# Performance work log

Measured on AMD Instinct MI355X. Metric: run time of the kernel, lower is better.

## Reference

```python
import jax, jax.numpy as jnp
import numpy as np

N = 6144          # active voxels / points
C = 96            # embed_channels
B = 2             # batch size
D = H = W = 32    # sparse spatial shape
K = 16            # PFAS kNN
DEPTH = 4
GRID_OPTS = np.array([[0.1, 0.1, 0.1], [0.4, 0.4, 0.4], [0.2, 0.2, 0.2]], dtype=np.float32)
BN_EPS = 1e-5


def _bn(x, g, b):
    # BatchNorm1d in training mode: batch stats over the point dim, biased var
    m = x.mean(0)
    v = jnp.var(x, axis=0)
    return (x - m) * jax.lax.rsqrt(v + BN_EPS) * g + b


def _seg_sum(x, seg):
    return jax.ops.segment_sum(x, seg, num_segments=N)


def _forward(indices, x, fp_w, fp_b, fp_g, fp_be, att_w1, att_b1, att_w2, att_b2,
             ff_w1, ff_b1, ff_g, ff_be, ff_w2, ff_b2, sa_w1, sa_b1, sa_w2, sa_b2,
             fj_w1, fj_b1, fj_g, fj_be, fj_w2, fj_b2,
             proj_w, proj_g, proj_be, lw_w, lw_g, lw_be, w_w, adp_w,
             fuse_w, fuse_g, fuse_be, conv1_w, bn1_g, bn1_be, conv2_w, bn2_g, bn2_be):
    # ---- CMPFE ----
    p = jax.nn.relu(_bn(x @ fp_w.T + fp_b, fp_g, fp_be))            # [N,9]
    cd, cl, nm = p[:, :3], p[:, 3:6], p[:, 6:9]

    def _att(f, i):
        h = jax.nn.relu(f @ att_w1[i].T + att_b1[i])
        return jax.nn.sigmoid(h @ att_w2[i].T + att_b2[i])

    enh = jnp.concatenate([cd, cl * _att(cl, 0), nm * _att(nm, 1)], axis=1)
    fu = jax.nn.relu(_bn(enh @ ff_w1.T + ff_b1, ff_g, ff_be)) @ ff_w2.T + ff_b2
    sem = jax.nn.sigmoid(jax.nn.relu(fu @ sa_w1.T + sa_b1) @ sa_w2.T + sa_b2)
    feat = fu * sem + x * (1.0 - sem)                               # new x.features

    # ---- PFAS: kNN geometry stats ----
    coord = indices[:, 1:].astype(jnp.float32)                      # [N,3]
    batch = indices[:, 0]
    sq = jnp.sum(coord * coord, axis=1)
    d2 = sq[:, None] + sq[None, :] - 2.0 * (coord @ coord.T)
    dist = jnp.sqrt(jnp.maximum(d2, 1e-12))
    same = batch[None, :] == batch[:, None]
    eye = jnp.eye(N, dtype=bool)
    dist = jnp.where(same & ~eye, dist, jnp.inf)
    neg_nd, idx = jax.lax.top_k(-dist, K)                           # K nearest
    nbr = coord[idx]                                                # [N,K,3]
    cent = nbr - nbr.mean(axis=1, keepdims=True)
    cov = jnp.einsum('nkd,nke->nde', cent, cent) / (K - 1)
    S = jnp.linalg.svd(cov, compute_uv=False)                       # [N,3] descending
    Sn = S / (S.sum(axis=1, keepdims=True) + 1e-6)
    linearity = Sn[:, 0:1] - (Sn[:, 1] + Sn[:, 2])[:, None]
    mean_dist = (-neg_nd).mean(axis=1, keepdims=True)
    density = 1.0 / (mean_dist + 1e-6)
    fl = jax.nn.relu(_bn(feat @ fj_w1.T + fj_b1, fj_g, fj_be)) @ fj_w2.T + fj_b2
    fp_ = jax.nn.softmax(fl, axis=1)
    tower = (density * 2.0 + fp_[:, 0:1]) / 3.0
    backg = (jnp.maximum(1.0 - linearity, 1.0 - density) + fp_[:, 1:2]) / 3.0
    line = (linearity * 2.0 + fp_[:, 2:3]) / 3.0
    go = jnp.asarray(GRID_OPTS)
    lg = go[2] * jnp.array([1.0, 1.0, 5.0], jnp.float32)            # last dim *5
    grid_sizes = tower * go[0] + backg * go[1] + line * lg + 1e-6   # [N,3]

    # ---- representative grids (N > 200 path) ----
    gm = grid_sizes.mean(axis=1)
    order = jnp.argsort(gm)
    reps = [grid_sizes[order[100:200]].mean(0),
            grid_sizes[order[::-1][:100]].mean(0),
            grid_sizes[order[:100]].mean(0)]

    # ---- voxel-grid clustering (torch_geometric voxel_grid + unique inverse) ----
    start = coord.min(axis=0)

    def _cluster(size):
        size = jnp.clip(size, 1e-6, None)
        c = jnp.clip(jnp.floor((coord - start) / size).astype(jnp.int64), 0, 4095)
        mx = c.max(axis=0) + 1
        ids = ((batch.astype(jnp.int64) * mx[0] + c[:, 0]) * mx[1] + c[:, 1]) * mx[2] + c[:, 2]
        _, inv = jnp.unique(ids, return_inverse=True, size=N, fill_value=0)
        return inv.reshape(-1)

    # ---- adaptive multi-branch scatter softmax aggregation ----
    branch_feats = []
    for i in range(DEPTH - 1):
        seg = _cluster(reps[i])
        cnt = jnp.maximum(_seg_sum(jnp.ones((N, 1), feat.dtype), seg), 1.0)
        pw = jax.nn.relu(_bn(feat @ lw_w[i].T, lw_g[i], lw_be[i]))
        pw = pw - (_seg_sum(pw, seg) / cnt)[seg]
        pw = pw @ w_w[i].T
        pw = jnp.exp(pw - pw.max())
        pw = pw / (_seg_sum(pw, seg)[seg] + 1e-6)
        pf = jax.nn.relu(_bn(feat @ proj_w[i].T, proj_g[i], proj_be[i])) * pw
        branch_feats.append(_seg_sum(pf, seg)[seg])
    adp = jax.nn.softmax(feat @ adp_w.T, axis=1)                    # [N,3]
    agg = jnp.einsum('nc,ncd->nd', adp, jnp.stack(branch_feats, 1))
    last = jax.nn.relu(_bn(feat @ proj_w[-1].T, proj_g[-1], proj_be[-1]))
    fused = jax.nn.relu(_bn(jnp.concatenate([last, agg], 1) @ fuse_w.T, fuse_g, fuse_be)) + feat
    res = fused

    # ---- submanifold sparse conv block (dense scatter form; inactive sites zero,
    #      outputs gathered only at active sites == SubMConv3d) ----
    bi, zi, yi, xi = indices[:, 0], indices[:, 1], indices[:, 2], indices[:, 3]

    def _subm(f, w):
        grid = jnp.zeros((B, D, H, W, C), f.dtype).at[bi, zi, yi, xi].set(f)
        o = jax.lax.conv_general_dilated(grid, w, (1, 1, 1), 'SAME',
                                         dimension_numbers=('NDHWC', 'DHWIO', 'NDHWC'))
        return o[bi, zi, yi, xi]

    f1 = jax.nn.relu(_bn(_subm(fused, conv1_w), bn1_g, bn1_be))
    f2 = _bn(_subm(f1, conv2_w), bn2_g, bn2_be)
    return jax.nn.relu(f2 + res)


def setup_inputs() -> dict:
    key = jax.random.key(0)
    ks = iter(jax.random.split(key, 64))

    def rn(*shape, s=0.05):
        return jax.random.normal(next(ks), shape, jnp.float32) * s

    # unique active voxel coordinates
    rng = np.random.default_rng(0)
    flat = rng.choice(B * D * H * W, size=N, replace=False)
    b = flat // (D * H * W)
    r = flat % (D * H * W)
    z = r // (H * W)
    y = (r % (H * W)) // W
    xw = r % W
    indices = jnp.asarray(np.stack([b, z, y, xw], 1).astype(np.int32))
    Ch = C // 2
    return {
        'x': jax.random.normal(next(ks), (N, C), jnp.float32),
        'indices': indices,
        'fp_w': rn(9, C), 'fp_b': rn(9), 'fp_g': jnp.ones(9), 'fp_be': jnp.zeros(9),
        'att_w1': rn(2, 16, 3), 'att_b1': rn(2, 16), 'att_w2': rn(2, 3, 16), 'att_b2': rn(2, 3),
        'ff_w1': rn(C, 9), 'ff_b1': rn(C), 'ff_g': jnp.ones(C), 'ff_be': jnp.zeros(C),
        'ff_w2': rn(C, C), 'ff_b2': rn(C),
        'sa_w1': rn(Ch, C), 'sa_b1': rn(Ch), 'sa_w2': rn(1, Ch), 'sa_b2': rn(1),
        'fj_w1': rn(64, C), 'fj_b1': rn(64), 'fj_g': jnp.ones(64), 'fj_be': jnp.zeros(64),
        'fj_w2': rn(3, 64), 'fj_b2': rn(3),
        'proj_w': rn(DEPTH, C, C), 'proj_g': jnp.ones((DEPTH, C)), 'proj_be': jnp.zeros((DEPTH, C)),
        'lw_w': rn(DEPTH - 1, C, C), 'lw_g': jnp.ones((DEPTH - 1, C)), 'lw_be': jnp.zeros((DEPTH - 1, C)),
        'w_w': rn(DEPTH - 1, C, C),
        'adp_w': rn(DEPTH - 1, C),
        'fuse_w': rn(C, 2 * C), 'fuse_g': jnp.ones(C), 'fuse_be': jnp.zeros(C),
        'conv1_w': rn(3, 3, 3, C, C), 'bn1_g': jnp.ones(C), 'bn1_be': jnp.zeros(C),
        'conv2_w': rn(3, 3, 3, C, C), 'bn2_g': jnp.ones(C), 'bn2_be': jnp.zeros(C),
    }


def reference(x, indices, fp_w, fp_b, fp_g, fp_be, att_w1, att_b1, att_w2, att_b2,
              ff_w1, ff_b1, ff_g, ff_be, ff_w2, ff_b2, sa_w1, sa_b1, sa_w2, sa_b2,
              fj_w1, fj_b1, fj_g, fj_be, fj_w2, fj_b2,
              proj_w, proj_g, proj_be, lw_w, lw_g, lw_be, w_w, adp_w,
              fuse_w, fuse_g, fuse_be, conv1_w, bn1_g, bn1_be, conv2_w, bn2_g, bn2_be):
    return _forward(indices, x, fp_w, fp_b, fp_g, fp_be, att_w1, att_b1, att_w2, att_b2,
                    ff_w1, ff_b1, ff_g, ff_be, ff_w2, ff_b2, sa_w1, sa_b1, sa_w2, sa_b2,
                    fj_w1, fj_b1, fj_g, fj_be, fj_w2, fj_b2,
                    proj_w, proj_g, proj_be, lw_w, lw_g, lw_be, w_w, adp_w,
                    fuse_w, fuse_g, fuse_be, conv1_w, bn1_g, bn1_be, conv2_w, bn2_g, bn2_be)
```

## Files before the change

### kernel.cpp

```cpp
#include <hip/hip_runtime.h>
#include <cstdint>

#define NPTS 6144
#define CH 96
#define NCELEM (NPTS*CH)
#define HTSZ 16384
#define NBALL 514

__device__ __forceinline__ unsigned fenc(float f){
  unsigned u = __float_as_uint(f);
  return (u & 0x80000000u) ? ~u : (u | 0x80000000u);
}
__device__ __forceinline__ float fdec(unsigned u){
  unsigned b = (u & 0x80000000u) ? (u & 0x7FFFFFFFu) : ~u;
  return __uint_as_float(b);
}

__device__ void eig3(double a00,double a01,double a02,double a11,double a12,double a22,
                     double &e0,double &e1,double &e2){
  double p1 = a01*a01 + a02*a02 + a12*a12;
  double q = (a00+a11+a22)/3.0;
  double b00=a00-q, b11=a11-q, b22=a22-q;
  double p2 = b00*b00 + b11*b11 + b22*b22 + 2.0*p1;
  if (p2 <= 1e-300){ e0=e1=e2=q; return; }
  double pp = sqrt(p2/6.0);
  double inv = 1.0/pp;
  double c00=b00*inv, c01=a01*inv, c02=a02*inv, c11=b11*inv, c12=a12*inv, c22=b22*inv;
  double det = c00*(c11*c22-c12*c12) - c01*(c01*c22-c12*c02) + c02*(c01*c12-c11*c02);
  double r = det*0.5;
  r = r < -1.0 ? -1.0 : (r > 1.0 ? 1.0 : r);
  double phi = acos(r)/3.0;
  e0 = q + 2.0*pp*cos(phi);
  e2 = q + 2.0*pp*cos(phi + 2.0943951023931953);
  e1 = 3.0*q - e0 - e2;
}

__global__ void k_setup0(int* __restrict__ zb, long zcount,
                         unsigned long long* __restrict__ htk, int* __restrict__ htv,
                         int* __restrict__ table, int* __restrict__ startmm){
  long i = (long)blockIdx.x*blockDim.x + threadIdx.x;
  long st = (long)gridDim.x*blockDim.x;
  for (long j=i; j<zcount; j+=st) zb[j] = 0;
  for (long j=i; j<3*HTSZ; j+=st){ htk[j] = ~0ull; htv[j] = 0x7fffffff; }
  for (long j=i; j<2*32768; j+=st) table[j] = -1;
  if (i < 3) startmm[i] = 0x7fffffff;
  else if (i < 6) startmm[i] = 0;
}
__global__ void __launch_bounds__(256) k_setup1(const int* __restrict__ ind,
                                                unsigned* __restrict__ packed,
                                                int* __restrict__ startmm,
                                                int* __restrict__ table,
                                                unsigned* __restrict__ ball){
  __shared__ int mn[3], mx[3];
  __shared__ int hcnt[32], hbase[32], hpos[32];
  int tid = threadIdx.x;
  if (blockIdx.x < 24){
    if (tid < 3){ mn[tid] = 0x7fffffff; mx[tid] = 0; }
    __syncthreads();
    int p = blockIdx.x*256 + tid;
    int b = ind[p*4], z = ind[p*4+1], y = ind[p*4+2], x = ind[p*4+3];
    packed[p] = (unsigned)((b<<15)|(z<<10)|(y<<5)|x);
    table[((b*32+z)*32+y)*32+x] = p;
    atomicMin(&mn[0], z); atomicMin(&mn[1], y); atomicMin(&mn[2], x);
    atomicMax(&mx[0], z); atomicMax(&mx[1], y); atomicMax(&mx[2], x);
    __syncthreads();
    if (tid < 3){
      atomicMin(&startmm[tid], mn[tid]);
      atomicMax(&startmm[3+tid], mx[tid]);
    }
  } else {
    if (tid < 32){ hcnt[tid] = 0; hpos[tid] = 0; }
    __syncthreads();
    for (int i=tid; i<1331; i+=256){
      int dz = i/121, rm = i - dz*121, dy = rm/11, dx = rm - dy*11;
      int a = dz-5, b = dy-5, c = dx-5;
      int d2 = a*a + b*b + c*c;
      if (d2 > 0 && d2 <= 25) atomicAdd(&hcnt[d2], 1);
    }
    __syncthreads();
    if (tid == 0){
      int acc = 0;
      for (int d=1; d<=25; ++d){ hbase[d] = acc; acc += hcnt[d]; }
    }
    __syncthreads();
    for (int i=tid; i<1331; i+=256){
      int dz = i/121, rm = i - dz*121, dy = rm/11, dx = rm - dy*11;
      int a = dz-5, b = dy-5, c = dx-5;
      int d2 = a*a + b*b + c*c;
      if (d2 > 0 && d2 <= 25){
        int pos = hbase[d2] + atomicAdd(&hpos[d2], 1);
        ball[pos] = ((unsigned)d2<<16)|((unsigned)dz<<10)|((unsigned)dy<<5)|(unsigned)dx;
      }
    }
  }
}

__global__ void __launch_bounds__(256) k_mm(
    const float* __restrict__ Abase, const float* __restrict__ Wbase,
    const float* __restrict__ biasBase, float* __restrict__ Obase,
    int CIN, int COUT,
    long sA, long sW, long sO, long sBias,
    const float* __restrict__ statsBase, long sStats,
    const float* __restrict__ gBase, const float* __restrict__ beBase, long sGB,
    const float* __restrict__ SsumBase, const int* __restrict__ segBase, const int* __restrict__ cntBase,
    unsigned* maxenc, int mode)
{
  int zb = blockIdx.y;
  const float* A = Abase + (long)zb*sA;
  const float* W = Wbase + (long)zb*sW;
  float* O = Obase + (long)zb*sO;
  const float* st = statsBase ? statsBase + (long)zb*sStats : nullptr;
  const float* g  = gBase ? gBase + (long)zb*sGB : nullptr;
  const float* be = beBase ? beBase + (long)zb*sGB : nullptr;
  const float* Ss = SsumBase ? SsumBase + (long)zb*NCELEM : nullptr;
  const int* seg  = segBase ? segBase + (long)zb*NPTS : nullptr;
  const int* cnt  = cntBase ? cntBase + (long)zb*NPTS : nullptr;

  __shared__ float Alt[96*34];
  __shared__ float Wlt[96*98];
  int tid = threadIdx.x;
  int r0 = blockIdx.x*32;
  for (int idx = tid; idx < CIN*COUT; idx += 256){
    int co = idx / CIN, k = idx - co*CIN;
    Wlt[k*98 + co] = W[idx];
  }
  for (int idx = tid; idx < 32*CIN; idx += 256){
    int ir = idx / CIN, k = idx - ir*CIN;
    int row = r0 + ir;
    float v = A[(long)row*CIN + k];
    if (mode >= 1) v = fmaxf((v - st[k*2])*st[k*2+1]*g[k] + be[k], 0.f);
    if (mode == 2){
      int s = seg[row];
      float cf = fmaxf((float)cnt[s], 1.f);
      v -= Ss[(long)s*CH + k] / cf;
    }
    Alt[k*34 + ir] = v;
  }
  __syncthreads();
  float lmax = -3.4e38f;
  if (COUT == 96){
    int rp = tid >> 4, cg = tid & 15;
    int co0 = cg*6;
    float acc0[6], acc1[6];
    #pragma unroll
    for (int j=0;j<6;++j){
      float b = biasBase ? biasBase[(long)zb*sBias + co0 + j] : 0.f;
      acc0[j] = b; acc1[j] = b;
    }
    int ra = 2*rp;
    for (int k=0;k<CIN;++k){
      float2 a  = *(const float2*)&Alt[k*34 + ra];
      float2 w0 = *(const float2*)&Wlt[k*98 + co0];
      float2 w1 = *(const float2*)&Wlt[k*98 + co0 + 2];
      float2 w2 = *(const float2*)&Wlt[k*98 + co0 + 4];
      acc0[0] = fmaf(a.x, w0.x, acc0[0]); acc1[0] = fmaf(a.y, w0.x, acc1[0]);
      acc0[1] = fmaf(a.x, w0.y, acc0[1]); acc1[1] = fmaf(a.y, w0.y, acc1[1]);
      acc0[2] = fmaf(a.x, w1.x, acc0[2]); acc1[2] = fmaf(a.y, w1.x, acc1[2]);
      acc0[3] = fmaf(a.x, w1.y, acc0[3]); acc1[3] = fmaf(a.y, w1.y, acc1[3]);
      acc0[4] = fmaf(a.x, w2.x, acc0[4]); acc1[4] = fmaf(a.y, w2.x, acc1[4]);
      acc0[5] = fmaf(a.x, w2.y, acc0[5]); acc1[5] = fmaf(a.y, w2.y, acc1[5]);
    }
    int rb = ra+1;
    #pragma unroll
    for (int j=0;j<6;++j){
      O[(long)(r0+ra)*96 + co0 + j] = acc0[j];
      O[(long)(r0+rb)*96 + co0 + j] = acc1[j];
      lmax = fmaxf(lmax, fmaxf(acc0[j], acc1[j]));
    }
  } else {
    for (int idx = tid; idx < 32*COUT; idx += 256){
      int ir = idx/COUT, co = idx - ir*COUT;
      float acc = biasBase ? biasBase[(long)zb*sBias + co] : 0.f;
      for (int k=0;k<CIN;++k) acc = fmaf(Alt[k*34+ir], Wlt[k*98+co], acc);
      O[(long)(r0+ir)*COUT + co] = acc;
      lmax = fmaxf(lmax, acc);
    }
  }
  if (maxenc){
    __shared__ float rmx[256];
    rmx[tid] = lmax; __syncthreads();
    for (int s2=128; s2>0; s2>>=1){
      if (tid < s2) rmx[tid] = fmaxf(rmx[tid], rmx[tid+s2]);
      __syncthreads();
    }
    if (tid == 0) atomicMax(&maxenc[zb], fenc(rmx[0]));
  }
}

__global__ void __launch_bounds__(256) k_mm_fuse(
    const float* __restrict__ tp3, const float* __restrict__ st,
    const float* __restrict__ pg3, const float* __restrict__ pbe3,
    const float* __restrict__ agg, const float* __restrict__ fw, float* __restrict__ tf)
{
  __shared__ float Alt[192*34];
  __shared__ float Wlt[96*98];
  int tid = threadIdx.x, r0 = blockIdx.x*32;
  for (int idx = tid; idx < 32*192; idx += 256){
    int ir = idx/192, k = idx - ir*192;
    int row = r0 + ir;
    float v;
    if (k < 96){
      v = tp3[(long)row*96 + k];
      v = fmaxf((v - st[k*2])*st[k*2+1]*pg3[k] + pbe3[k], 0.f);
    } else {
      v = agg[(long)row*96 + (k-96)];
    }
    Alt[k*34 + ir] = v;
  }
  int rp = tid >> 4, cg = tid & 15, co0 = cg*6;
  float acc0[6] = {0,0,0,0,0,0}, acc1[6] = {0,0,0,0,0,0};
  int ra = 2*rp, rb = ra+1;
  for (int h=0; h<2; ++h){
    __syncthreads();
    for (int idx = tid; idx < 96*96; idx += 256){
      int co = idx/96, k = idx - co*96;
      Wlt[k*98+co] = fw[(long)co*192 + h*96 + k];
    }
    __syncthreads();
    for (int k=0;k<96;++k){
      float2 a  = *(const float2*)&Alt[(h*96 + k)*34 + ra];
      float2 w0 = *(const float2*)&Wlt[k*98 + co0];
      float2 w1 = *(const float2*)&Wlt[k*98 + co0 + 2];
      float2 w2 = *(const float2*)&Wlt[k*98 + co0 + 4];
      acc0[0] = fmaf(a.x, w0.x, acc0[0]); acc1[0] = fmaf(a.y, w0.x, acc1[0]);
      acc0[1] = fmaf(a.x, w0.y, acc0[1]); acc1[1] = fmaf(a.y, w0.y, acc1[1]);
      acc0[2] = fmaf(a.x, w1.x, acc0[2]); acc1[2] = fmaf(a.y, w1.x, acc1[2]);
      acc0[3] = fmaf(a.x, w1.y, acc0[3]); acc1[3] = fmaf(a.y, w1.y, acc1[3]);
      acc0[4] = fmaf(a.x, w2.x, acc0[4]); acc1[4] = fmaf(a.y, w2.x, acc1[4]);
      acc0[5] = fmaf(a.x, w2.y, acc0[5]); acc1[5] = fmaf(a.y, w2.y, acc1[5]);
    }
  }
  #pragma unroll
  for (int j=0;j<6;++j){
    tf[(long)(r0+ra)*96 + co0 + j] = acc0[j];
    tf[(long)(r0+rb)*96 + co0 + j] = acc1[j];
  }
}

__global__ void k_stats(const float* __restrict__ Abase, long sA, int COLS,
                        float* __restrict__ statsBase, long sStats){
  int col = blockIdx.x, zb = blockIdx.y;
  const float* A = Abase + (long)zb*sA;
  double s = 0.0, q = 0.0;
  for (int r = threadIdx.x; r < NPTS; r += 256){
    double v = (double)A[(long)r*COLS + col];
    s += v; q += v*v;
  }
  __shared__ double ls[256], lq[256];
  ls[threadIdx.x] = s; lq[threadIdx.x] = q; __syncthreads();
  for (int t=128; t>0; t>>=1){
    if (threadIdx.x < t){ ls[threadIdx.x] += ls[threadIdx.x+t]; lq[threadIdx.x] += lq[threadIdx.x+t]; }
    __syncthreads();
  }
  if (threadIdx.x == 0){
    double mean = ls[0]/NPTS;
    double var = lq[0]/NPTS - mean*mean;
    float* stp = statsBase + (long)zb*sStats + col*2;
    stp[0] = (float)mean;
    stp[1] = (float)(1.0/sqrt(var + 1e-5));
  }
}

__global__ void k_p_att_enh(const float* __restrict__ t9, const float* __restrict__ st,
                            const float* __restrict__ fg, const float* __restrict__ fbe,
                            const float* __restrict__ aw1, const float* __restrict__ ab1,
                            const float* __restrict__ aw2, const float* __restrict__ ab2,
                            float* __restrict__ enh){
  int p = blockIdx.x*blockDim.x + threadIdx.x;
  if (p >= NPTS) return;
  float pp[9];
  #pragma unroll
  for (int c=0;c<9;++c){
    float v = t9[p*9+c];
    pp[c] = fmaxf((v - st[c*2])*st[c*2+1]*fg[c] + fbe[c], 0.f);
  }
  float eo[9];
  eo[0]=pp[0]; eo[1]=pp[1]; eo[2]=pp[2];
  #pragma unroll
  for (int i=0;i<2;++i){
    const float* w1 = aw1 + i*48;
    const float* b1 = ab1 + i*16;
    const float* w2 = aw2 + i*48;
    const float* b2 = ab2 + i*3;
    const float* f = pp + 3 + i*3;
    float h[16];
    #pragma unroll
    for (int j=0;j<16;++j){
      float s = b1[j];
      #pragma unroll
      for (int k=0;k<3;++k) s = fmaf(f[k], w1[j*3+k], s);
      h[j] = fmaxf(s, 0.f);
    }
    #pragma unroll
    for (int o=0;o<3;++o){
      float s = b2[o];
      #pragma unroll
      for (int j=0;j<16;++j) s = fmaf(h[j], w2[o*16+j], s);
      float a = 1.f/(1.f + expf(-s));
      eo[3+i*3+o] = f[o]*a;
    }
  }
  #pragma unroll
  for (int c=0;c<9;++c) enh[p*9+c] = eo[c];
}

__global__ void __launch_bounds__(256) k_sem_feat(
    const float* __restrict__ fu, const float* __restrict__ x,
    const float* __restrict__ w1, const float* __restrict__ b1,
    const float* __restrict__ w2, const float* __restrict__ b2,
    float* __restrict__ feat){
  int wid = (blockIdx.x*blockDim.x + threadIdx.x) >> 6;
  int lane = threadIdx.x & 63;
  if (wid >= NPTS) return;
  const float* fr = fu + (long)wid*96;
  float partial = 0.f;
  if (lane < 48){
    float h = b1[lane];
    for (int k=0;k<96;++k) h = fmaf(fr[k], w1[lane*96+k], h);
    h = fmaxf(h, 0.f);
    partial = h * w2[lane];
  }
  for (int m=32; m; m>>=1) partial += __shfl_xor(partial, m);
  float sem = 1.f/(1.f + expf(-(partial + b2[0])));
  for (int c=lane; c<96; c+=64){
    float f = fr[c];
    feat[(long)wid*96+c] = f*sem + x[(long)wid*96+c]*(1.f - sem);
  }
}

__global__ void __launch_bounds__(256) k_knn(const unsigned* __restrict__ packed,
                                             const int* __restrict__ table,
                                             const unsigned* __restrict__ ball,
                                             float* __restrict__ density, float* __restrict__ linearity){
  __shared__ unsigned pk[NPTS];
  for (int i=threadIdx.x; i<NPTS; i+=256) pk[i] = packed[i];
  __syncthreads();
  int pid = blockIdx.x*4 + (threadIdx.x>>6);
  int lane = threadIdx.x & 63;
  unsigned mypc = pk[pid];
  int myb = (int)(mypc>>15);
  int mz = (int)((mypc>>10)&31), my_=(int)((mypc>>5)&31), mx_=(int)(mypc&31);
  unsigned s[16];
  #pragma unroll
  for (int t=0;t<16;++t) s[t] = 0xFFFFFFFFu;
  int cnt = 0;
  const int tbase = myb*32768;
  for (int it=0; it<9; ++it){
    int i = lane + it*64;
    if (i < NBALL){
      unsigned e = ball[i];
      int d2 = (int)(e >> 16);
      int dz = (int)((e>>10)&31) - 5;
      int dy = (int)((e>>5)&31) - 5;
      int dx = (int)(e&31) - 5;
      int zz = mz+dz, yy = my_+dy, xx = mx_+dx;
      if ((unsigned)zz < 32u && (unsigned)yy < 32u && (unsigned)xx < 32u){
        int j = table[tbase + (zz*32+yy)*32+xx];
        if (j >= 0){
          ++cnt;
          unsigned key = ((unsigned)d2<<13) | (unsigned)j;
          if (key < s[15]){
            s[15] = key;
            #pragma unroll
            for (int t=15;t>0;--t){
              unsigned a = s[t-1], b = s[t];
              unsigned lo = a<b?a:b, hi = a<b?b:a;
              s[t-1]=lo; s[t]=hi;
            }
          }
        }
      }
    }
    int nxt = (it+1)*64;
    if (nxt >= NBALL) break;
    int tot = cnt;
    for (int m=32; m; m>>=1) tot += __shfl_xor(tot, m);
    unsigned dlast = ball[nxt-1] >> 16;
    unsigned dnext = ball[nxt] >> 16;
    if (tot >= 16 && dnext > dlast) break;
  }
  int tot = cnt;
  for (int m=32; m; m>>=1) tot += __shfl_xor(tot, m);
  if (tot < 16){
    #pragma unroll
    for (int t=0;t<16;++t) s[t] = 0xFFFFFFFFu;
    for (int it=0; it<96; ++it){
      int j = lane + it*64;
      unsigned pc = pk[j];
      if (j != pid && (int)(pc>>15) == myb){
        int dz = (int)((pc>>10)&31) - mz;
        int dy = (int)((pc>>5)&31) - my_;
        int dx = (int)(pc&31) - mx_;
        unsigned d2 = (unsigned)(dz*dz + dy*dy + dx*dx);
        unsigned key = (d2<<13) | (unsigned)j;
        if (key < s[15]){
          s[15] = key;
          #pragma unroll
          for (int t=15;t>0;--t){
            unsigned a = s[t-1], b = s[t];
            unsigned lo = a<b?a:b, hi = a<b?b:a;
            s[t-1]=lo; s[t]=hi;
          }
        }
      }
    }
  }
  float sdist = 0.f;
  int sz=0,sy=0,sx=0,szz=0,syy=0,sxx=0,szy=0,szx=0,syx=0;
  for (int r=0;r<16;++r){
    unsigned m = s[0];
    #pragma unroll
    for (int w=32; w; w>>=1){
      unsigned o = (unsigned)__shfl_xor((int)m, w);
      m = m<o ? m : o;
    }
    bool own = (s[0] == m);
    #pragma unroll
    for (int t=0;t<15;++t) s[t] = own ? s[t+1] : s[t];
    if (own) s[15] = 0xFFFFFFFFu;
    unsigned idx = m & 8191u;
    unsigned d2 = m >> 13;
    sdist += sqrtf((float)d2);
    unsigned pc = pk[idx];
    int nz=(int)((pc>>10)&31), ny=(int)((pc>>5)&31), nx=(int)(pc&31);
    sz+=nz; sy+=ny; sx+=nx;
    szz+=nz*nz; syy+=ny*ny; sxx+=nx*nx; szy+=nz*ny; szx+=nz*nx; syx+=ny*nx;
  }
  if (lane == 0){
    double m0 = sz/16.0, m1 = sy/16.0, m2 = sx/16.0;
    float c00 = (float)(((double)szz - 16.0*m0*m0)/15.0);
    float c11 = (float)(((double)syy - 16.0*m1*m1)/15.0);
    float c22 = (float)(((double)sxx - 16.0*m2*m2)/15.0);
    float c01 = (float)(((double)szy - 16.0*m0*m1)/15.0);
    float c02 = (float)(((double)szx - 16.0*m0*m2)/15.0);
    float c12 = (float)(((double)syx - 16.0*m1*m2)/15.0);
    double e0,e1,e2;
    eig3((double)c00,(double)c01,(double)c02,(double)c11,(double)c12,(double)c22, e0,e1,e2);
    float s0 = (float)fabs(e0), s1 = (float)fabs(e1), s2 = (float)fabs(e2);
    float den = s0 + s1 + s2 + 1e-6f;
    float sn0 = s0/den, sn1 = s1/den, sn2 = s2/den;
    linearity[pid] = sn0 - (sn1 + sn2);
    float md = sdist * (1.f/16.f);
    density[pid] = 1.f/(md + 1e-6f);
  }
}

__global__ void k_geo(const float* __restrict__ t64, const float* __restrict__ st,
                      const float* __restrict__ fg, const float* __restrict__ fbe,
                      const float* __restrict__ w2, const float* __restrict__ b2,
                      const float* __restrict__ density, const float* __restrict__ linearity,
                      float* __restrict__ gsz, float* __restrict__ gm){
  int p = blockIdx.x*blockDim.x + threadIdx.x;
  if (p >= NPTS) return;
  float fl[3];
  #pragma unroll
  for (int o=0;o<3;++o) fl[o] = b2[o];
  for (int k=0;k<64;++k){
    float v = t64[(long)p*64+k];
    v = fmaxf((v - st[k*2])*st[k*2+1]*fg[k] + fbe[k], 0.f);
    #pragma unroll
    for (int o=0;o<3;++o) fl[o] = fmaf(v, w2[o*64+k], fl[o]);
  }
  float mx = fmaxf(fl[0], fmaxf(fl[1], fl[2]));
  float e0 = expf(fl[0]-mx), e1 = expf(fl[1]-mx), e2 = expf(fl[2]-mx);
  float es = e0+e1+e2;
  float p0 = e0/es, p1 = e1/es, p2 = e2/es;
  float den = density[p], lin = linearity[p];
  float tw = (den*2.f + p0)/3.f;
  float bg = (fmaxf(1.f-lin, 1.f-den) + p1)/3.f;
  float ln = (lin*2.f + p2)/3.f;
  float g0 = tw*0.1f + bg*0.4f + ln*0.2f + 1e-6f;
  float g1 = tw*0.1f + bg*0.4f + ln*0.2f + 1e-6f;
  float g2 = tw*0.1f + bg*0.4f + ln*1.0f + 1e-6f;
  gsz[p*3+0]=g0; gsz[p*3+1]=g1; gsz[p*3+2]=g2;
  gm[p] = (g0+g1+g2)/3.f;
}

#define RNKCHUNK 768
__global__ void __launch_bounds__(256) k_rank(const float* __restrict__ gm, int* __restrict__ rank){
  __shared__ unsigned long long lk[RNKCHUNK];
  int j0 = blockIdx.y*RNKCHUNK;
  for (int i=threadIdx.x; i<RNKCHUNK; i+=256){
    int j = j0 + i;
    lk[i] = (((unsigned long long)fenc(gm[j]))<<13) | (unsigned long long)j;
  }
  __syncthreads();
  int p = blockIdx.x*256 + threadIdx.x;
  unsigned long long myk = (((unsigned long long)fenc(gm[p]))<<13) | (unsigned long long)p;
  int cnt = 0;
  #pragma unroll 4
  for (int i=0; i<RNKCHUNK; ++i) cnt += (lk[i] < myk) ? 1 : 0;
  atomicAdd(&rank[p], cnt);
}
__global__ void __launch_bounds__(256) k_scatter_reps(const int* __restrict__ rank,
                                                      const float* __restrict__ gsz,
                                                      float* __restrict__ bkt,
                                                      int* __restrict__ done,
                                                      float* __restrict__ reps){
  __shared__ int lastf;
  int p = blockIdx.x*256 + threadIdx.x;
  int r = rank[p];
  int zb = -1, t = 0;
  if (r < 100){ zb = 2; t = r; }
  else if (r < 200){ zb = 0; t = r - 100; }
  else if (r >= NPTS-100){ zb = 1; t = r - (NPTS-100); }
  if (zb >= 0){
    #pragma unroll
    for (int d=0; d<3; ++d) bkt[(zb*100 + t)*3 + d] = gsz[p*3+d];
  }
  __threadfence();
  __syncthreads();
  if (threadIdx.x == 0) lastf = (atomicAdd(done, 1) == 23) ? 1 : 0;
  __syncthreads();
  if (lastf){
    __threadfence();
    int i = threadIdx.x;
    if (i < 9){
      int z = i/3, d = i - z*3;
      double s = 0.0;
      for (int tt=0; tt<100; ++tt) s += (double)bkt[(z*100 + tt)*3 + d];
      reps[i] = (float)(s/100.0);
    }
  }
}

__global__ void k_cluster(const int* __restrict__ ind, const float* __restrict__ reps,
                          const int* __restrict__ startmm, long long* __restrict__ ids){
  int z = blockIdx.y;
  int p = blockIdx.x*blockDim.x + threadIdx.x;
  if (p >= NPTS) return;
  long long mxp[3]; int cc[3];
  #pragma unroll
  for (int d=0; d<3; ++d){
    float sizev = fmaxf(reps[z*3+d], 1e-6f);
    float cf = floorf(((float)ind[p*4+1+d] - (float)startmm[d]) / sizev);
    int ci = (int)cf;
    ci = ci < 0 ? 0 : (ci > 4095 ? 4095 : ci);
    cc[d] = ci;
    float cfm = floorf(((float)startmm[3+d] - (float)startmm[d]) / sizev);
    int cm = (int)cfm;
    cm = cm < 0 ? 0 : (cm > 4095 ? 4095 : cm);
    mxp[d] = (long long)cm + 1;
  }
  long long b = ind[p*4];
  ids[(long)z*NPTS + p] = ((b*mxp[0] + cc[0])*mxp[1] + cc[1])*mxp[2] + cc[2];
}

__device__ __forceinline__ int ht_hash(unsigned long long id){
  unsigned long long h = id * 0x9E3779B97F4A7C15ull;
  return (int)(h >> 49) & (HTSZ-1);
}
__global__ void k_seg_build(const long long* __restrict__ ids,
                            unsigned long long* __restrict__ keys, int* __restrict__ vals){
  int z = blockIdx.y;
  int p = blockIdx.x*blockDim.x + threadIdx.x;
  if (p >= NPTS) return;
  unsigned long long id = (unsigned long long)ids[(long)z*NPTS + p];
  unsigned long long* K = keys + (long)z*HTSZ;
  int* V = vals + (long)z*HTSZ;
  int slot = ht_hash(id);
  while (true){
    unsigned long long prev = atomicCAS(&K[slot], ~0ull, id);
    if (prev == ~0ull || prev == id){ atomicMin(&V[slot], p); break; }
    slot = (slot + 1) & (HTSZ-1);
  }
}
__global__ void k_seg_lookup(const long long* __restrict__ ids,
                             const unsigned long long* __restrict__ keys, const int* __restrict__ vals,
                             int* __restrict__ seg, int* __restrict__ cnt){
  int z = blockIdx.y;
  int p = blockIdx.x*blockDim.x + threadIdx.x;
  if (p >= NPTS) return;
  unsigned long long id = (unsigned long long)ids[(long)z*NPTS + p];
  const unsigned long long* K = keys + (long)z*HTSZ;
  int slot = ht_hash(id);
  while (K[slot] != id) slot = (slot + 1) & (HTSZ-1);
  int rep = vals[(long)z*HTSZ + slot];
  seg[(long)z*NPTS + p] = rep;
  atomicAdd(&cnt[(long)z*NPTS + rep], 1);
}

__global__ void k_pw_accum(const float* __restrict__ tlw, const float* __restrict__ stats,
                           const float* __restrict__ g, const float* __restrict__ be,
                           const int* __restrict__ seg, float* __restrict__ S){
  int z = blockIdx.y;
  int idx = blockIdx.x*blockDim.x + threadIdx.x;
  int p = idx/CH, c = idx - p*CH;
  const float* st = stats + z*192;
  float v = tlw[(long)z*NCELEM + idx];
  v = fmaxf((v - st[c*2])*st[c*2+1]*g[z*CH+c] + be[z*CH+c], 0.f);
  atomicAdd(&S[(long)z*NCELEM + (long)seg[(long)z*NPTS+p]*CH + c], v);
}
__global__ void k_exp_accum(const float* __restrict__ pw2, const unsigned* __restrict__ maxenc,
                            const int* __restrict__ seg, float* __restrict__ E){
  int z = blockIdx.y;
  int idx = blockIdx.x*blockDim.x + threadIdx.x;
  int p = idx/CH, c = idx - p*CH;
  float mv = fdec(maxenc[z]);
  float v = expf(pw2[(long)z*NCELEM + idx] - mv);
  atomicAdd(&E[(long)z*NCELEM + (long)seg[(long)z*NPTS+p]*CH + c], v);
}
__global__ void k_pf_accum(const float* __restrict__ tp, const float* __restrict__ stats,
                           const float* __restrict__ pg, const float* __restrict__ pbe,
                           const float* __restrict__ pw2, const unsigned* __restrict__ maxenc,
                           const int* __restrict__ seg, const float* __restrict__ E,
                           float* __restrict__ F){
  int z = blockIdx.y;
  int idx = blockIdx.x*blockDim.x + threadIdx.x;
  int p = idx/CH, c = idx - p*CH;
  const float* st = stats + z*192;
  float v = tp[(long)z*NCELEM + idx];
  v = fmaxf((v - st[c*2])*st[c*2+1]*pg[z*CH+c] + pbe[z*CH+c], 0.f);
  float mv = fdec(maxenc[z]);
  int sg = seg[(long)z*NPTS+p];
  float w = expf(pw2[(long)z*NCELEM + idx] - mv) / (E[(long)z*NCELEM + (long)sg*CH + c] + 1e-6f);
  atomicAdd(&F[(long)z*NCELEM + (long)sg*CH + c], v*w);
}
__global__ void __launch_bounds__(256) k_adp_agg(
    const float* __restrict__ feat, const float* __restrict__ aw,
    const float* __restrict__ F, const int* __restrict__ seg,
    float* __restrict__ agg){
  __shared__ float ladp[32][3];
  __shared__ int lseg[32][3];
  int tid = threadIdx.x;
  int p0 = blockIdx.x*32;
  if (tid < 96){
    int pl = tid/3, z = tid - pl*3;
    const float* fr = feat + (long)(p0+pl)*CH;
    float a = 0.f;
    for (int k=0;k<CH;++k) a = fmaf(fr[k], aw[z*CH+k], a);
    ladp[pl][z] = a;
    lseg[pl][z] = seg[(long)z*NPTS + (p0+pl)];
  }
  __syncthreads();
  if (tid < 32){
    float a0 = ladp[tid][0], a1 = ladp[tid][1], a2 = ladp[tid][2];
    float m = fmaxf(a0, fmaxf(a1,a2));
    float e0 = expf(a0-m), e1 = expf(a1-m), e2 = expf(a2-m);
    float s = e0+e1+e2;
    ladp[tid][0]=e0/s; ladp[tid][1]=e1/s; ladp[tid][2]=e2/s;
  }
  __syncthreads();
  for (int e = tid; e < 32*CH; e += 256){
    int pl = e/CH, c = e - pl*CH;
    float s = 0.f;
    #pragma unroll
    for (int z=0;z<3;++z)
      s = fmaf(ladp[pl][z], F[(long)z*NCELEM + (long)lseg[pl][z]*CH + c], s);
    agg[(long)p0*CH + e] = s;
  }
}

__global__ void k_zero(int* p, long n){
  long i = (long)blockIdx.x*blockDim.x + threadIdx.x;
  long st = (long)gridDim.x*blockDim.x;
  for (; i < n; i += st) p[i] = 0;
}
__global__ void k_fused(const float* __restrict__ tf, const float* __restrict__ st,
                        const float* __restrict__ fg, const float* __restrict__ fbe,
                        const float* __restrict__ feat, float* __restrict__ fused){
  int idx = blockIdx.x*blockDim.x + threadIdx.x;
  int c = idx % CH;
  float v = tf[idx];
  v = fmaxf((v - st[c*2])*st[c*2+1]*fg[c] + fbe[c], 0.f);
  fused[idx] = v + feat[idx];
}
__global__ void k_bnrelu(const float* __restrict__ a, const float* __restrict__ st,
                         const float* __restrict__ g, const float* __restrict__ be,
                         float* __restrict__ o){
  int idx = blockIdx.x*blockDim.x + threadIdx.x;
  int c = idx % CH;
  float v = a[idx];
  o[idx] = fmaxf((v - st[c*2])*st[c*2+1]*g[c] + be[c], 0.f);
}

__global__ void __launch_bounds__(256) k_nbrlist(const int* __restrict__ ind,
                                                 const int* __restrict__ table,
                                                 int* __restrict__ nbrtab,
                                                 int* __restrict__ tapcnt,
                                                 int* __restrict__ ptlist){
  __shared__ int pb[256], pz[256], py[256], px[256];
  __shared__ int lcnt[27], lbase[27], lpos[27];
  int tid = threadIdx.x;
  if (tid < 27){ lcnt[tid] = 0; lpos[tid] = 0; }
  int p0 = blockIdx.x*256;
  pb[tid] = ind[(p0+tid)*4];
  pz[tid] = ind[(p0+tid)*4+1];
  py[tid] = ind[(p0+tid)*4+2];
  px[tid] = ind[(p0+tid)*4+3];
  __syncthreads();
  int base = blockIdx.x*6912;
  int qv[27];
  #pragma unroll 1
  for (int j = 0; j < 27; ++j){
    int i = tid + j*256;
    int pl = i/27, tap = i - pl*27;
    int dz = tap/9 - 1;
    int rm = tap % 9;
    int dy = rm/3 - 1, dx = rm%3 - 1;
    int z = pz[pl]+dz, y = py[pl]+dy, x = px[pl]+dx;
    int q = -1;
    if ((unsigned)z < 32u && (unsigned)y < 32u && (unsigned)x < 32u)
      q = table[((pb[pl]*32+z)*32+y)*32+x];
    qv[j] = q;
    nbrtab[base + i] = q;
    if (q >= 0) atomicAdd(&lcnt[tap], 1);
  }
  __syncthreads();
  if (tid < 27) lbase[tid] = atomicAdd(&tapcnt[tid], lcnt[tid]);
  __syncthreads();
  #pragma unroll 1
  for (int j = 0; j < 27; ++j){
    int q = qv[j];
    if (q >= 0){
      int i = tid + j*256;
      int tap = i % 27;
      int p = p0 + i/27;
      int pos = lbase[tap] + atomicAdd(&lpos[tap], 1);
      ptlist[tap*NPTS + pos] = (p<<16) | q;
    }
  }
}
__global__ void __launch_bounds__(256) k_conv_gemm(
    const float* __restrict__ src, const float* __restrict__ Wc,
    const int* __restrict__ tapcnt, const int* __restrict__ ptlist,
    const float* __restrict__ bnst, const float* __restrict__ bng,
    const float* __restrict__ bnbe, const float* __restrict__ res,
    int fmode, float* __restrict__ part){
  int tap = blockIdx.y;
  int n = tapcnt[tap];
  int r0 = blockIdx.x*32;
  if (r0 >= n) return;
  __shared__ float Alt[96*34];
  __shared__ float Wlt[96*98];
  __shared__ int pqs[32];
  int tid = threadIdx.x;
  if (tid < 32){
    int r = r0 + tid;
    pqs[tid] = (r < n) ? ptlist[tap*NPTS + r] : -1;
  }
  __syncthreads();
  for (int idx4 = tid; idx4 < 2304; idx4 += 256){
    int ci = idx4/24, c4 = idx4 - ci*24;
    float4 w = ((const float4*)(Wc + ((long)tap*96 + ci)*96))[c4];
    float* d = &Wlt[ci*98 + c4*4];
    d[0]=w.x; d[1]=w.y; d[2]=w.z; d[3]=w.w;
  }
  for (int idx4 = tid; idx4 < 32*24; idx4 += 256){
    int ir = idx4/24, c4 = idx4 - ir*24;
    int pq = pqs[ir];
    float4 s4 = make_float4(0.f,0.f,0.f,0.f);
    if (pq >= 0){
      int q = pq & 0xFFFF;
      s4 = ((const float4*)(src + (long)q*CH))[c4];
      if (fmode){
        int c0 = c4*4;
        float vx = fmaxf((s4.x - bnst[(c0+0)*2])*bnst[(c0+0)*2+1]*bng[c0+0] + bnbe[c0+0], 0.f);
        float vy = fmaxf((s4.y - bnst[(c0+1)*2])*bnst[(c0+1)*2+1]*bng[c0+1] + bnbe[c0+1], 0.f);
        float vz = fmaxf((s4.z - bnst[(c0+2)*2])*bnst[(c0+2)*2+1]*bng[c0+2] + bnbe[c0+2], 0.f);
        float vw = fmaxf((s4.w - bnst[(c0+3)*2])*bnst[(c0+3)*2+1]*bng[c0+3] + bnbe[c0+3], 0.f);
        if (fmode == 2){
          const float* rr = res + (long)q*CH + c0;
          vx += rr[0]; vy += rr[1]; vz += rr[2]; vw += rr[3];
        }
        s4 = make_float4(vx,vy,vz,vw);
      }
    }
    int k0 = c4*4;
    Alt[(k0+0)*34 + ir] = s4.x;
    Alt[(k0+1)*34 + ir] = s4.y;
    Alt[(k0+2)*34 + ir] = s4.z;
    Alt[(k0+3)*34 + ir] = s4.w;
  }
  __syncthreads();
  int rp = tid >> 4, cg = tid & 15;
  int co0 = cg*6;
  int ra = 2*rp, rb = ra+1;
  float acc0[6]={0,0,0,0,0,0}, acc1[6]={0,0,0,0,0,0};
  for (int k=0;k<96;++k){
    float2 a  = *(const float2*)&Alt[k*34 + ra];
    float2 w0 = *(const float2*)&Wlt[k*98 + co0];
    float2 w1 = *(const float2*)&Wlt[k*98 + co0 + 2];
    float2 w2 = *(const float2*)&Wlt[k*98 + co0 + 4];
    acc0[0] = fmaf(a.x, w0.x, acc0[0]); acc1[0] = fmaf(a.y, w0.x, acc1[0]);
    acc0[1] = fmaf(a.x, w0.y, acc0[1]); acc1[1] = fmaf(a.y, w0.y, acc1[1]);
    acc0[2] = fmaf(a.x, w1.x, acc0[2]); acc1[2] = fmaf(a.y, w1.x, acc1[2]);
    acc0[3] = fmaf(a.x, w1.y, acc0[3]); acc1[3] = fmaf(a.y, w1.y, acc1[3]);
    acc0[4] = fmaf(a.x, w2.x, acc0[4]); acc1[4] = fmaf(a.y, w2.x, acc1[4]);
    acc0[5] = fmaf(a.x, w2.y, acc0[5]); acc1[5] = fmaf(a.y, w2.y, acc1[5]);
  }
  int pa = pqs[ra], pb2 = pqs[rb];
  if (pa >= 0){
    float* o = part + ((long)(pa>>16)*27 + tap)*CH + co0;
    #pragma unroll
    for (int j=0;j<6;++j) o[j] = acc0[j];
  }
  if (pb2 >= 0){
    float* o = part + ((long)(pb2>>16)*27 + tap)*CH + co0;
    #pragma unroll
    for (int j=0;j<6;++j) o[j] = acc1[j];
  }
}
__global__ void __launch_bounds__(256) k_conv_sum(const int* __restrict__ nbrtab,
                                                  const float* __restrict__ part,
                                                  float* __restrict__ out){
  int idx = blockIdx.x*256 + threadIdx.x;
  int p = idx/24, c4 = idx - p*24;
  const int* nt = nbrtab + p*27;
  float4 acc = make_float4(0.f,0.f,0.f,0.f);
  for (int tap=0; tap<27; ++tap){
    if (nt[tap] >= 0){
      float4 v = ((const float4*)part)[((long)p*27 + tap)*24 + c4];
      acc.x += v.x; acc.y += v.y; acc.z += v.z; acc.w += v.w;
    }
  }
  ((float4*)out)[idx] = acc;
}
__global__ void __launch_bounds__(256) k_conv_gemm_atomic(
    const float* __restrict__ src, const float* __restrict__ Wc,
    const int* __restrict__ tapcnt, const int* __restrict__ ptlist,
    float* __restrict__ out){
  int tap = blockIdx.y;
  int n = tapcnt[tap];
  int r0 = blockIdx.x*32;
  if (r0 >= n) return;
  __shared__ float Al[32*97];
  __shared__ float Wl[96*97];
  __shared__ int pqs[32];
  int tid = threadIdx.x;
  if (tid < 32){
    int r = r0 + tid;
    pqs[tid] = (r < n) ? ptlist[tap*NPTS + r] : -1;
  }
  __syncthreads();
  for (int idx4 = tid; idx4 < 2304; idx4 += 256){
    int ci = idx4/24, c4 = idx4 - ci*24;
    float4 w = ((const float4*)(Wc + ((long)tap*96 + ci)*96))[c4];
    float* d = &Wl[ci*97 + c4*4];
    d[0]=w.x; d[1]=w.y; d[2]=w.z; d[3]=w.w;
  }
  for (int idx4 = tid; idx4 < 32*24; idx4 += 256){
    int ir = idx4/24, c4 = idx4 - ir*24;
    int pq = pqs[ir];
    float4 s = make_float4(0.f,0.f,0.f,0.f);
    if (pq >= 0){
      int q = pq & 0xFFFF;
      s = ((const float4*)(src + (long)q*CH))[c4];
    }
    float* d = &Al[ir*97 + c4*4];
    d[0]=s.x; d[1]=s.y; d[2]=s.z; d[3]=s.w;
  }
  __syncthreads();
  int rp = tid >> 4, cg = tid & 15;
  int co0 = cg*6;
  int ra = 2*rp, rb = ra+1;
  float acc0[6]={0,0,0,0,0,0}, acc1[6]={0,0,0,0,0,0};
  for (int k=0;k<96;++k){
    float a0 = Al[ra*97+k], a1 = Al[rb*97+k];
    #pragma unroll
    for (int j=0;j<6;++j){
      float w = Wl[k*97+co0+j];
      acc0[j] = fmaf(a0, w, acc0[j]);
      acc1[j] = fmaf(a1, w, acc1[j]);
    }
  }
  int pa = pqs[ra], pb = pqs[rb];
  if (pa >= 0){
    float* o = out + (long)(pa>>16)*CH + co0;
    #pragma unroll
    for (int j=0;j<6;++j) atomicAdd(&o[j], acc0[j]);
  }
  if (pb >= 0){
    float* o = out + (long)(pb>>16)*CH + co0;
    #pragma unroll
    for (int j=0;j<6;++j) atomicAdd(&o[j], acc1[j]);
  }
}
__global__ void k_final(const float* __restrict__ c2, const float* __restrict__ st12,
                        const float* __restrict__ g2, const float* __restrict__ be2,
                        const float* __restrict__ tf, const float* __restrict__ st10,
                        const float* __restrict__ fg, const float* __restrict__ fbe,
                        const float* __restrict__ feat, float* __restrict__ out){
  int idx = blockIdx.x*blockDim.x + threadIdx.x;
  int c = idx % CH;
  float fsd = fmaxf((tf[idx] - st10[c*2])*st10[c*2+1]*fg[c] + fbe[c], 0.f) + feat[idx];
  float v = (c2[idx] - st12[c*2])*st12[c*2+1]*g2[c] + be2[c];
  out[idx] = fmaxf(v + fsd, 0.f);
}

extern "C" void kernel_launch(void* const* d_in, const int* in_sizes, int n_in,
                              void* d_out, int out_size, void* d_ws, size_t ws_size,
                              hipStream_t stream)
{
  const float* x      = (const float*)d_in[0];
  const int*   ind    = (const int*)  d_in[1];
  const float* fp_w   = (const float*)d_in[2];
  const float* fp_b   = (const float*)d_in[3];
  const float* fp_g   = (const float*)d_in[4];
  const float* fp_be  = (const float*)d_in[5];
  const float* att_w1 = (const float*)d_in[6];
  const float* att_b1 = (const float*)d_in[7];
  const float* att_w2 = (const float*)d_in[8];
  const float* att_b2 = (const float*)d_in[9];
  const float* ff_w1  = (const float*)d_in[10];
  const float* ff_b1  = (const float*)d_in[11];
  const float* ff_g   = (const float*)d_in[12];
  const float* ff_be  = (const float*)d_in[13];
  const float* ff_w2  = (const float*)d_in[14];
  const float* ff_b2  = (const float*)d_in[15];
  const float* sa_w1  = (const float*)d_in[16];
  const float* sa_b1  = (const float*)d_in[17];
  const float* sa_w2  = (const float*)d_in[18];
  const float* sa_b2  = (const float*)d_in[19];
  const float* fj_w1  = (const float*)d_in[20];
  const float* fj_b1  = (const float*)d_in[21];
  const float* fj_g   = (const float*)d_in[22];
  const float* fj_be  = (const float*)d_in[23];
  const float* fj_w2  = (const float*)d_in[24];
  const float* fj_b2  = (const float*)d_in[25];
  const float* proj_w = (const float*)d_in[26];
  const float* proj_g = (const float*)d_in[27];
  const float* proj_be= (const float*)d_in[28];
  const float* lw_w   = (const float*)d_in[29];
  const float* lw_g   = (const float*)d_in[30];
  const float* lw_be  = (const float*)d_in[31];
  const float* w_w    = (const float*)d_in[32];
  const float* adp_w  = (const float*)d_in[33];
  const float* fuse_w = (const float*)d_in[34];
  const float* fuse_g = (const float*)d_in[35];
  const float* fuse_be= (const float*)d_in[36];
  const float* conv1_w= (const float*)d_in[37];
  const float* bn1_g  = (const float*)d_in[38];
  const float* bn1_be = (const float*)d_in[39];
  const float* conv2_w= (const float*)d_in[40];
  const float* bn2_g  = (const float*)d_in[41];
  const float* bn2_be = (const float*)d_in[42];
  float* outp = (float*)d_out;
  (void)in_sizes; (void)n_in; (void)out_size;

  char* ws = (char*)d_ws;
  size_t off = 0;
  auto alloc = [&](size_t bytes)->size_t{
    off = (off + 255) & ~(size_t)255;
    size_t o = off; off += bytes; return o;
  };
  const size_t FNC = (size_t)NCELEM*4;
  size_t o_packed = alloc((size_t)NPTS*4);
  size_t o_start  = alloc(32);
  size_t o_ball   = alloc((size_t)NBALL*4);
  size_t o_dens   = alloc((size_t)NPTS*4);
  size_t o_lin    = alloc((size_t)NPTS*4);
  size_t o_t9     = alloc((size_t)NPTS*9*4);
  size_t o_enh    = alloc((size_t)NPTS*9*4);
  size_t o_gm     = alloc((size_t)NPTS*4);
  size_t o_gsz    = alloc((size_t)NPTS*3*4);
  size_t o_reps   = alloc(16*4);
  size_t o_bkt    = alloc((size_t)3*100*3*4);
  size_t o_ids    = alloc((size_t)3*NPTS*8);
  size_t o_seg    = alloc((size_t)3*NPTS*4);
  size_t o_table  = alloc((size_t)65536*4);
  size_t o_nbr    = alloc((size_t)NPTS*27*4);
  size_t o_ptlist = alloc((size_t)27*NPTS*4);
  size_t o_t64    = alloc((size_t)NPTS*64*4);
  size_t o_stats  = alloc((size_t)13*192*4);
  size_t o_htk    = alloc((size_t)3*HTSZ*8);
  size_t o_htv    = alloc((size_t)3*HTSZ*4);
  size_t o_S      = alloc(3*FNC);
  size_t o_E      = alloc(3*FNC);
  size_t o_F      = alloc(3*FNC);
  size_t o_cnt    = alloc((size_t)3*NPTS*4);
  size_t o_rank   = alloc((size_t)NPTS*4);
  size_t o_tapcnt = alloc(32*4);
  size_t o_done   = alloc(16);
  size_t o_maxenc = alloc(16*4);
  size_t zend = off;
  size_t o_T96 = alloc(FNC);
  size_t o_fu  = alloc(FNC);
  size_t o_feat= alloc(FNC);
  size_t o_tlw = alloc(3*FNC);
  size_t o_pw2 = alloc(3*FNC);
  size_t o_tp  = alloc(4*FNC);
  size_t o_agg = alloc(FNC);
  size_t o_tf  = alloc(FNC);
  size_t o_fsd = alloc(FNC);
  size_t o_c1  = alloc(FNC);
  size_t o_f1  = alloc(FNC);
  size_t o_c2  = alloc(FNC);
  size_t o_part = alloc((size_t)NPTS*27*CH*4);
  bool use_part = (off <= ws_size);

  float* stats = (float*)(ws + o_stats);
  long zcount = (long)((zend - o_S)/4);

  k_setup0<<<dim3(2048), dim3(256), 0, stream>>>((int*)(ws+o_S), zcount,
      (unsigned long long*)(ws+o_htk), (int*)(ws+o_htv), (int*)(ws+o_table), (int*)(ws+o_start));
  k_setup1<<<dim3(25), 256, 0, stream>>>(ind, (unsigned*)(ws+o_packed),
      (int*)(ws+o_start), (int*)(ws+o_table), (unsigned*)(ws+o_ball));

  k_mm<<<dim3(192,1), 256, 0, stream>>>(x, fp_w, fp_b, (float*)(ws+o_t9), 96, 9,
      0,0,0,0, nullptr,0, nullptr,nullptr,0, nullptr,nullptr,nullptr, nullptr, 0);
  k_stats<<<dim3(9,1), 256, 0, stream>>>((float*)(ws+o_t9), 0, 9, stats+0*192, 0);
  k_p_att_enh<<<dim3(24), 256, 0, stream>>>((float*)(ws+o_t9), stats+0*192, fp_g, fp_be,
      att_w1, att_b1, att_w2, att_b2, (float*)(ws+o_enh));

  k_mm<<<dim3(192,1), 256, 0, stream>>>((float*)(ws+o_enh), ff_w1, ff_b1, (float*)(ws+o_T96), 9, 96,
      0,0,0,0, nullptr,0, nullptr,nullptr,0, nullptr,nullptr,nullptr, nullptr, 0);
  k_stats<<<dim3(96,1), 256, 0, stream>>>((float*)(ws+o_T96), 0, 96, stats+1*192, 0);
  k_mm<<<dim3(192,1), 256, 0, stream>>>((float*)(ws+o_T96), ff_w2, ff_b2, (float*)(ws+o_fu), 96, 96,
      0,0,0,0, stats+1*192,0, ff_g, ff_be,0, nullptr,nullptr,nullptr, nullptr, 1);

  k_sem_feat<<<dim3(1536), 256, 0, stream>>>((float*)(ws+o_fu), x, sa_w1, sa_b1, sa_w2, sa_b2,
      (float*)(ws+o_feat));

  k_knn<<<dim3(1536), 256, 0, stream>>>((unsigned*)(ws+o_packed), (int*)(ws+o_table),
      (unsigned*)(ws+o_ball), (float*)(ws+o_dens), (float*)(ws+o_lin));

  k_mm<<<dim3(192,1), 256, 0, stream>>>((float*)(ws+o_feat), fj_w1, fj_b1, (float*)(ws+o_t64), 96, 64,
      0,0,0,0, nullptr,0, nullptr,nullptr,0, nullptr,nullptr,nullptr, nullptr, 0);
  k_stats<<<dim3(64,1), 256, 0, stream>>>((float*)(ws+o_t64), 0, 64, stats+2*192, 0);
  k_geo<<<dim3(24), 256, 0, stream>>>((float*)(ws+o_t64), stats+2*192, fj_g, fj_be, fj_w2, fj_b2,
      (float*)(ws+o_dens), (float*)(ws+o_lin), (float*)(ws+o_gsz), (float*)(ws+o_gm));

  k_rank<<<dim3(24,8), 256, 0, stream>>>((float*)(ws+o_gm), (int*)(ws+o_rank));
  k_scatter_reps<<<dim3(24), 256, 0, stream>>>((int*)(ws+o_rank), (float*)(ws+o_gsz),
      (float*)(ws+o_bkt), (int*)(ws+o_done), (float*)(ws+o_reps));

  k_cluster<<<dim3(24,3), 256, 0, stream>>>(ind, (float*)(ws+o_reps), (int*)(ws+o_start),
      (long long*)(ws+o_ids));
  k_seg_build<<<dim3(24,3), 256, 0, stream>>>((long long*)(ws+o_ids),
      (unsigned long long*)(ws+o_htk), (int*)(ws+o_htv));
  k_seg_lookup<<<dim3(24,3), 256, 0, stream>>>((long long*)(ws+o_ids),
      (unsigned long long*)(ws+o_htk), (int*)(ws+o_htv), (int*)(ws+o_seg), (int*)(ws+o_cnt));

  k_mm<<<dim3(192,3), 256, 0, stream>>>((float*)(ws+o_feat), lw_w, nullptr, (float*)(ws+o_tlw), 96, 96,
      0, 96*96, NCELEM, 0, nullptr,0, nullptr,nullptr,0, nullptr,nullptr,nullptr, nullptr, 0);
  k_stats<<<dim3(96,3), 256, 0, stream>>>((float*)(ws+o_tlw), NCELEM, 96, stats+3*192, 192);
  k_pw_accum<<<dim3(2304,3), 256, 0, stream>>>((float*)(ws+o_tlw), stats+3*192, lw_g, lw_be,
      (int*)(ws+o_seg), (float*)(ws+o_S));
  k_mm<<<dim3(192,3), 256, 0, stream>>>((float*)(ws+o_tlw), w_w, nullptr, (float*)(ws+o_pw2), 96, 96,
      NCELEM, 96*96, NCELEM, 0, stats+3*192,192, lw_g, lw_be,96,
      (float*)(ws+o_S), (int*)(ws+o_seg), (int*)(ws+o_cnt), (unsigned*)(ws+o_maxenc), 2);
  k_exp_accum<<<dim3(2304,3), 256, 0, stream>>>((float*)(ws+o_pw2), (unsigned*)(ws+o_maxenc),
      (int*)(ws+o_seg), (float*)(ws+o_E));
  k_mm<<<dim3(192,4), 256, 0, stream>>>((float*)(ws+o_feat), proj_w, nullptr, (float*)(ws+o_tp), 96, 96,
      0, 96*96, NCELEM, 0, nullptr,0, nullptr,nullptr,0, nullptr,nullptr,nullptr, nullptr, 0);
  k_stats<<<dim3(96,4), 256, 0, stream>>>((float*)(ws+o_tp), NCELEM, 96, stats+6*192, 192);
  k_pf_accum<<<dim3(2304,3), 256, 0, stream>>>((float*)(ws+o_tp), stats+6*192, proj_g, proj_be,
      (float*)(ws+o_pw2), (unsigned*)(ws+o_maxenc), (int*)(ws+o_seg), (float*)(ws+o_E), (float*)(ws+o_F));
  k_adp_agg<<<dim3(192), 256, 0, stream>>>((float*)(ws+o_feat), adp_w, (float*)(ws+o_F),
      (int*)(ws+o_seg), (float*)(ws+o_agg));

  k_mm_fuse<<<dim3(192), 256, 0, stream>>>((float*)(ws+o_tp) + (size_t)3*NCELEM, stats+9*192,
      proj_g + 3*96, proj_be + 3*96, (float*)(ws+o_agg), fuse_w, (float*)(ws+o_tf));
  k_stats<<<dim3(96,1), 256, 0, stream>>>((float*)(ws+o_tf), 0, 96, stats+10*192, 0);

  k_nbrlist<<<dim3(24), 256, 0, stream>>>(ind, (int*)(ws+o_table), (int*)(ws+o_nbr),
      (int*)(ws+o_tapcnt), (int*)(ws+o_ptlist));
  if (use_part){
    k_conv_gemm<<<dim3(192,27), 256, 0, stream>>>((float*)(ws+o_tf), conv1_w,
        (int*)(ws+o_tapcnt), (int*)(ws+o_ptlist),
        stats+10*192, fuse_g, fuse_be, (float*)(ws+o_feat), 2, (float*)(ws+o_part));
    k_conv_sum<<<dim3(NPTS*24/256), 256, 0, stream>>>((int*)(ws+o_nbr), (float*)(ws+o_part),
        (float*)(ws+o_c1));
    k_stats<<<dim3(96,1), 256, 0, stream>>>((float*)(ws+o_c1), 0, 96, stats+11*192, 0);
    k_conv_gemm<<<dim3(192,27), 256, 0, stream>>>((float*)(ws+o_c1), conv2_w,
        (int*)(ws+o_tapcnt), (int*)(ws+o_ptlist),
        stats+11*192, bn1_g, bn1_be, nullptr, 1, (float*)(ws+o_part));
    k_conv_sum<<<dim3(NPTS*24/256), 256, 0, stream>>>((int*)(ws+o_nbr), (float*)(ws+o_part),
        (float*)(ws+o_c2));
  } else {
    k_fused<<<dim3(2304), 256, 0, stream>>>((float*)(ws+o_tf), stats+10*192, fuse_g, fuse_be,
        (float*)(ws+o_feat), (float*)(ws+o_fsd));
    k_zero<<<dim3(2304), dim3(256), 0, stream>>>((int*)(ws+o_c1), NCELEM);
    k_conv_gemm_atomic<<<dim3(192,27), 256, 0, stream>>>((float*)(ws+o_fsd), conv1_w,
        (int*)(ws+o_tapcnt), (int*)(ws+o_ptlist), (float*)(ws+o_c1));
    k_stats<<<dim3(96,1), 256, 0, stream>>>((float*)(ws+o_c1), 0, 96, stats+11*192, 0);
    k_bnrelu<<<dim3(2304), 256, 0, stream>>>((float*)(ws+o_c1), stats+11*192, bn1_g, bn1_be,
        (float*)(ws+o_f1));
    k_zero<<<dim3(2304), dim3(256), 0, stream>>>((int*)(ws+o_c2), NCELEM);
    k_conv_gemm_atomic<<<dim3(192,27), 256, 0, stream>>>((float*)(ws+o_f1), conv2_w,
        (int*)(ws+o_tapcnt), (int*)(ws+o_ptlist), (float*)(ws+o_c2));
  }
  k_stats<<<dim3(96,1), 256, 0, stream>>>((float*)(ws+o_c2), 0, 96, stats+12*192, 0);
  k_final<<<dim3(2304), 256, 0, stream>>>((float*)(ws+o_c2), stats+12*192, bn2_g, bn2_be,
      (float*)(ws+o_tf), stats+10*192, fuse_g, fuse_be, (float*)(ws+o_feat), outp);
}
```

Baseline: 486.6 us.

## Fuse BatchNorm statistic accumulation into producer GEMM epilogues and inline cluster ids

Removes most separate k_stats launches. The GEMM, fuse-GEMM and conv-sum kernels now accumulate per-channel sums and sums of squares, first in shared-memory float atomics and then in global double atomics. Consumers derive mean and rstd from the raw double sums and cache them in shared memory. The k_cluster kernel and its ids buffer are dropped, with cluster ids recomputed inside the hash build and lookup kernels. This saves launches and full re-reads of activations, at the cost of atomic contention and E[x^2]-mean^2 variance computed from per-block float partial sums.

New measurement: 516.7 us. +6.2%, slower.

```diff
diff --git a/kernel.cpp b/kernel.cpp
--- a/kernel.cpp
+++ b/kernel.cpp
@@ -14,6 +14,11 @@
 __device__ __forceinline__ float fdec(unsigned u){
   unsigned b = (u & 0x80000000u) ? (u & 0x7FFFFFFFu) : ~u;
   return __uint_as_float(b);
+}
+__device__ __forceinline__ float2 bnstat(const double* __restrict__ st, int c){
+  double mean = st[c*2] / (double)NPTS;
+  double var  = st[c*2+1] / (double)NPTS - mean*mean;
+  return make_float2((float)mean, (float)(1.0/sqrt(var + 1e-5)));
 }
 
 __device__ void eig3(double a00,double a01,double a02,double a11,double a12,double a22,
@@ -100,26 +105,35 @@
     const float* __restrict__ biasBase, float* __restrict__ Obase,
     int CIN, int COUT,
     long sA, long sW, long sO, long sBias,
-    const float* __restrict__ statsBase, long sStats,
+    const double* __restrict__ statsBase, long sStats,
     const float* __restrict__ gBase, const float* __restrict__ beBase, long sGB,
     const float* __restrict__ SsumBase, const int* __restrict__ segBase, const int* __restrict__ cntBase,
-    unsigned* maxenc, int mode)
+    unsigned* maxenc, int mode, double* statsumBase)
 {
   int zb = blockIdx.y;
   const float* A = Abase + (long)zb*sA;
   const float* W = Wbase + (long)zb*sW;
   float* O = Obase + (long)zb*sO;
-  const float* st = statsBase ? statsBase + (long)zb*sStats : nullptr;
+  const double* st = statsBase ? statsBase + (long)zb*sStats : nullptr;
   const float* g  = gBase ? gBase + (long)zb*sGB : nullptr;
   const float* be = beBase ? beBase + (long)zb*sGB : nullptr;
   const float* Ss = SsumBase ? SsumBase + (long)zb*NCELEM : nullptr;
   const int* seg  = segBase ? segBase + (long)zb*NPTS : nullptr;
   const int* cnt  = cntBase ? cntBase + (long)zb*NPTS : nullptr;
+  double* ssum = statsumBase ? statsumBase + (long)zb*192 : nullptr;
 
   __shared__ float Alt[96*34];
   __shared__ float Wlt[96*98];
+  __shared__ float lms[192];
+  __shared__ float lsum[96], lsq[96];
   int tid = threadIdx.x;
   int r0 = blockIdx.x*32;
+  if (tid < 96){ lsum[tid] = 0.f; lsq[tid] = 0.f; }
+  if (mode >= 1 && tid < CIN){
+    float2 ms = bnstat(st, tid);
+    lms[tid*2] = ms.x; lms[tid*2+1] = ms.y;
+  }
+  __syncthreads();
   for (int idx = tid; idx < CIN*COUT; idx += 256){
     int co = idx / CIN, k = idx - co*CIN;
     Wlt[k*98 + co] = W[idx];
@@ -128,7 +142,7 @@
     int ir = idx / CIN, k = idx - ir*CIN;
     int row = r0 + ir;
     float v = A[(long)row*CIN + k];
-    if (mode >= 1) v = fmaxf((v - st[k*2])*st[k*2+1]*g[k] + be[k], 0.f);
+    if (mode >= 1) v = fmaxf((v - lms[k*2])*lms[k*2+1]*g[k] + be[k], 0.f);
     if (mode == 2){
       int s = seg[row];
       float cf = fmaxf((float)cnt[s], 1.f);
@@ -167,6 +181,13 @@
       O[(long)(r0+rb)*96 + co0 + j] = acc1[j];
       lmax = fmaxf(lmax, fmaxf(acc0[j], acc1[j]));
     }
+    if (ssum){
+      #pragma unroll
+      for (int j=0;j<6;++j){
+        atomicAdd(&lsum[co0+j], acc0[j] + acc1[j]);
+        atomicAdd(&lsq[co0+j],  acc0[j]*acc0[j] + acc1[j]*acc1[j]);
+      }
+    }
   } else {
     for (int idx = tid; idx < 32*COUT; idx += 256){
       int ir = idx/COUT, co = idx - ir*COUT;
@@ -174,6 +195,17 @@
       for (int k=0;k<CIN;++k) acc = fmaf(Alt[k*34+ir], Wlt[k*98+co], acc);
       O[(long)(r0+ir)*COUT + co] = acc;
       lmax = fmaxf(lmax, acc);
+      if (ssum){
+        atomicAdd(&lsum[co], acc);
+        atomicAdd(&lsq[co], acc*acc);
+      }
+    }
+  }
+  if (ssum){
+    __syncthreads();
+    if (tid < COUT){
+      atomicAdd(&ssum[tid*2],   (double)lsum[tid]);
+      atomicAdd(&ssum[tid*2+1], (double)lsq[tid]);
     }
   }
   if (maxenc){
@@ -188,20 +220,27 @@
 }
 
 __global__ void __launch_bounds__(256) k_mm_fuse(
-    const float* __restrict__ tp3, const float* __restrict__ st,
+    const float* __restrict__ tp3, const double* __restrict__ st,
     const float* __restrict__ pg3, const float* __restrict__ pbe3,
-    const float* __restrict__ agg, const float* __restrict__ fw, float* __restrict__ tf)
+    const float* __restrict__ agg, const float* __restrict__ fw, float* __restrict__ tf,
+    double* __restrict__ tfsum)
 {
   __shared__ float Alt[192*34];
   __shared__ float Wlt[96*98];
+  __shared__ float lscr[192];
   int tid = threadIdx.x, r0 = blockIdx.x*32;
+  if (tid < 96){
+    float2 ms = bnstat(st, tid);
+    lscr[tid*2] = ms.x; lscr[tid*2+1] = ms.y;
+  }
+  __syncthreads();
   for (int idx = tid; idx < 32*192; idx += 256){
     int ir = idx/192, k = idx - ir*192;
     int row = r0 + ir;
     float v;
     if (k < 96){
       v = tp3[(long)row*96 + k];
-      v = fmaxf((v - st[k*2])*st[k*2+1]*pg3[k] + pbe3[k], 0.f);
+      v = fmaxf((v - lscr[k*2])*lscr[k*2+1]*pg3[k] + pbe3[k], 0.f);
     } else {
       v = agg[(long)row*96 + (k-96)];
     }
@@ -235,10 +274,23 @@
     tf[(long)(r0+ra)*96 + co0 + j] = acc0[j];
     tf[(long)(r0+rb)*96 + co0 + j] = acc1[j];
   }
+  __syncthreads();
+  if (tid < 96){ lscr[tid] = 0.f; lscr[96+tid] = 0.f; }
+  __syncthreads();
+  #pragma unroll
+  for (int j=0;j<6;++j){
+    atomicAdd(&lscr[co0+j],    acc0[j] + acc1[j]);
+    atomicAdd(&lscr[96+co0+j], acc0[j]*acc0[j] + acc1[j]*acc1[j]);
+  }
+  __syncthreads();
+  if (tid < 96){
+    atomicAdd(&tfsum[tid*2],   (double)lscr[tid]);
+    atomicAdd(&tfsum[tid*2+1], (double)lscr[96+tid]);
+  }
 }
 
 __global__ void k_stats(const float* __restrict__ Abase, long sA, int COLS,
-                        float* __restrict__ statsBase, long sStats){
+                        double* __restrict__ statsBase, long sStats){
   int col = blockIdx.x, zb = blockIdx.y;
   const float* A = Abase + (long)zb*sA;
   double s = 0.0, q = 0.0;
@@ -253,26 +305,30 @@
     __syncthreads();
   }
   if (threadIdx.x == 0){
-    double mean = ls[0]/NPTS;
-    double var = lq[0]/NPTS - mean*mean;
-    float* stp = statsBase + (long)zb*sStats + col*2;
-    stp[0] = (float)mean;
-    stp[1] = (float)(1.0/sqrt(var + 1e-5));
-  }
-}
-
-__global__ void k_p_att_enh(const float* __restrict__ t9, const float* __restrict__ st,
+    double* stp = statsBase + (long)zb*sStats + col*2;
+    stp[0] = ls[0];
+    stp[1] = lq[0];
+  }
+}
+
+__global__ void k_p_att_enh(const float* __restrict__ t9, const double* __restrict__ st,
                             const float* __restrict__ fg, const float* __restrict__ fbe,
                             const float* __restrict__ aw1, const float* __restrict__ ab1,
                             const float* __restrict__ aw2, const float* __restrict__ ab2,
                             float* __restrict__ enh){
+  __shared__ float lms[18];
+  if (threadIdx.x < 9){
+    float2 ms = bnstat(st, threadIdx.x);
+    lms[threadIdx.x*2] = ms.x; lms[threadIdx.x*2+1] = ms.y;
+  }
+  __syncthreads();
   int p = blockIdx.x*blockDim.x + threadIdx.x;
   if (p >= NPTS) return;
   float pp[9];
   #pragma unroll
   for (int c=0;c<9;++c){
     float v = t9[p*9+c];
-    pp[c] = fmaxf((v - st[c*2])*st[c*2+1]*fg[c] + fbe[c], 0.f);
+    pp[c] = fmaxf((v - lms[c*2])*lms[c*2+1]*fg[c] + fbe[c], 0.f);
   }
   float eo[9];
   eo[0]=pp[0]; eo[1]=pp[1]; eo[2]=pp[2];
@@ -445,11 +501,17 @@
   }
 }
 
-__global__ void k_geo(const float* __restrict__ t64, const float* __restrict__ st,
+__global__ void k_geo(const float* __restrict__ t64, const double* __restrict__ st,
                       const float* __restrict__ fg, const float* __restrict__ fbe,
                       const float* __restrict__ w2, const float* __restrict__ b2,
                       const float* __restrict__ density, const float* __restrict__ linearity,
                       float* __restrict__ gsz, float* __restrict__ gm){
+  __shared__ float lms[128];
+  if (threadIdx.x < 64){
+    float2 ms = bnstat(st, threadIdx.x);
+    lms[threadIdx.x*2] = ms.x; lms[threadIdx.x*2+1] = ms.y;
+  }
+  __syncthreads();
   int p = blockIdx.x*blockDim.x + threadIdx.x;
   if (p >= NPTS) return;
   float fl[3];
@@ -457,7 +519,7 @@
   for (int o=0;o<3;++o) fl[o] = b2[o];
   for (int k=0;k<64;++k){
     float v = t64[(long)p*64+k];
-    v = fmaxf((v - st[k*2])*st[k*2+1]*fg[k] + fbe[k], 0.f);
+    v = fmaxf((v - lms[k*2])*lms[k*2+1]*fg[k] + fbe[k], 0.f);
     #pragma unroll
     for (int o=0;o<3;++o) fl[o] = fmaf(v, w2[o*64+k], fl[o]);
   }
@@ -524,11 +586,9 @@
   }
 }
 
-__global__ void k_cluster(const int* __restrict__ ind, const float* __restrict__ reps,
-                          const int* __restrict__ startmm, long long* __restrict__ ids){
-  int z = blockIdx.y;
-  int p = blockIdx.x*blockDim.x + threadIdx.x;
-  if (p >= NPTS) return;
+__device__ __forceinline__ unsigned long long cluster_id(
+    const int* __restrict__ ind, const float* __restrict__ reps,
+    const int* __restrict__ startmm, int z, int p){
   long long mxp[3]; int cc[3];
   #pragma unroll
   for (int d=0; d<3; ++d){
@@ -543,19 +603,20 @@
     mxp[d] = (long long)cm + 1;
   }
   long long b = ind[p*4];
-  ids[(long)z*NPTS + p] = ((b*mxp[0] + cc[0])*mxp[1] + cc[1])*mxp[2] + cc[2];
+  return (unsigned long long)(((b*mxp[0] + cc[0])*mxp[1] + cc[1])*mxp[2] + cc[2]);
 }
 
 __device__ __forceinline__ int ht_hash(unsigned long long id){
   unsigned long long h = id * 0x9E3779B97F4A7C15ull;
   return (int)(h >> 49) & (HTSZ-1);
 }
-__global__ void k_seg_build(const long long* __restrict__ ids,
+__global__ void k_seg_build(const int* __restrict__ ind, const float* __restrict__ reps,
+                            const int* __restrict__ startmm,
                             unsigned long long* __restrict__ keys, int* __restrict__ vals){
   int z = blockIdx.y;
   int p = blockIdx.x*blockDim.x + threadIdx.x;
   if (p >= NPTS) return;
-  unsigned long long id = (unsigned long long)ids[(long)z*NPTS + p];
+  unsigned long long id = cluster_id(ind, reps, startmm, z, p);
   unsigned long long* K = keys + (long)z*HTSZ;
   int* V = vals + (long)z*HTSZ;
   int slot = ht_hash(id);
@@ -565,13 +626,14 @@
     slot = (slot + 1) & (HTSZ-1);
   }
 }
-__global__ void k_seg_lookup(const long long* __restrict__ ids,
+__global__ void k_seg_lookup(const int* __restrict__ ind, const float* __restrict__ reps,
+                             const int* __restrict__ startmm,
                              const unsigned long long* __restrict__ keys, const int* __restrict__ vals,
                              int* __restrict__ seg, int* __restrict__ cnt){
   int z = blockIdx.y;
   int p = blockIdx.x*blockDim.x + threadIdx.x;
   if (p >= NPTS) return;
-  unsigned long long id = (unsigned long long)ids[(long)z*NPTS + p];
+  unsigned long long id = cluster_id(ind, reps, startmm, z, p);
   const unsigned long long* K = keys + (long)z*HTSZ;
   int slot = ht_hash(id);
   while (K[slot] != id) slot = (slot + 1) & (HTSZ-1);
@@ -580,15 +642,20 @@
   atomicAdd(&cnt[(long)z*NPTS + rep], 1);
 }
 
-__global__ void k_pw_accum(const float* __restrict__ tlw, const float* __restrict__ stats,
+__global__ void k_pw_accum(const float* __restrict__ tlw, const double* __restrict__ stats,
                            const float* __restrict__ g, const float* __restrict__ be,
                            const int* __restrict__ seg, float* __restrict__ S){
   int z = blockIdx.y;
+  __shared__ float lms[192];
+  if (threadIdx.x < 96){
+    float2 ms = bnstat(stats + (long)z*192, threadIdx.x);
+    lms[threadIdx.x*2] = ms.x; lms[threadIdx.x*2+1] = ms.y;
+  }
+  __syncthreads();
   int idx = blockIdx.x*blockDim.x + threadIdx.x;
   int p = idx/CH, c = idx - p*CH;
-  const float* st = stats + z*192;
   float v = tlw[(long)z*NCELEM + idx];
-  v = fmaxf((v - st[c*2])*st[c*2+1]*g[z*CH+c] + be[z*CH+c], 0.f);
+  v = fmaxf((v - lms[c*2])*lms[c*2+1]*g[z*CH+c] + be[z*CH+c], 0.f);
   atomicAdd(&S[(long)z*NCELEM + (long)seg[(long)z*NPTS+p]*CH + c], v);
 }
 __global__ void k_exp_accum(const float* __restrict__ pw2, const unsigned* __restrict__ maxenc,
@@ -600,17 +667,22 @@
   float v = expf(pw2[(long)z*NCELEM + idx] - mv);
   atomicAdd(&E[(long)z*NCELEM + (long)seg[(long)z*NPTS+p]*CH + c], v);
 }
-__global__ void k_pf_accum(const float* __restrict__ tp, const float* __restrict__ stats,
+__global__ void k_pf_accum(const float* __restrict__ tp, const double* __restrict__ stats,
                            const float* __restrict__ pg, const float* __restrict__ pbe,
                            const float* __restrict__ pw2, const unsigned* __restrict__ maxenc,
                            const int* __restrict__ seg, const float* __restrict__ E,
                            float* __restrict__ F){
   int z = blockIdx.y;
+  __shared__ float lms[192];
+  if (threadIdx.x < 96){
+    float2 ms = bnstat(stats + (long)z*192, threadIdx.x);
+    lms[threadIdx.x*2] = ms.x; lms[threadIdx.x*2+1] = ms.y;
+  }
+  __syncthreads();
   int idx = blockIdx.x*blockDim.x + threadIdx.x;
   int p = idx/CH, c = idx - p*CH;
-  const float* st = stats + z*192;
   float v = tp[(long)z*NCELEM + idx];
-  v = fmaxf((v - st[c*2])*st[c*2+1]*pg[z*CH+c] + pbe[z*CH+c], 0.f);
+  v = fmaxf((v - lms[c*2])*lms[c*2+1]*pg[z*CH+c] + pbe[z*CH+c], 0.f);
   float mv = fdec(maxenc[z]);
   int sg = seg[(long)z*NPTS+p];
   float w = expf(pw2[(long)z*NCELEM + idx] - mv) / (E[(long)z*NCELEM + (long)sg*CH + c] + 1e-6f);
@@ -656,22 +728,24 @@
   long st = (long)gridDim.x*blockDim.x;
   for (; i < n; i += st) p[i] = 0;
 }
-__global__ void k_fused(const float* __restrict__ tf, const float* __restrict__ st,
+__global__ void k_fused(const float* __restrict__ tf, const double* __restrict__ st,
                         const float* __restrict__ fg, const float* __restrict__ fbe,
                         const float* __restrict__ feat, float* __restrict__ fused){
   int idx = blockIdx.x*blockDim.x + threadIdx.x;
   int c = idx % CH;
+  float2 ms = bnstat(st, c);
   float v = tf[idx];
-  v = fmaxf((v - st[c*2])*st[c*2+1]*fg[c] + fbe[c], 0.f);
+  v = fmaxf((v - ms.x)*ms.y*fg[c] + fbe[c], 0.f);
   fused[idx] = v + feat[idx];
 }
-__global__ void k_bnrelu(const float* __restrict__ a, const float* __restrict__ st,
+__global__ void k_bnrelu(const float* __restrict__ a, const double* __restrict__ st,
                          const float* __restrict__ g, const float* __restrict__ be,
                          float* __restrict__ o){
   int idx = blockIdx.x*blockDim.x + threadIdx.x;
   int c = idx % CH;
+  float2 ms = bnstat(st, c);
   float v = a[idx];
-  o[idx] = fmaxf((v - st[c*2])*st[c*2+1]*g[c] + be[c], 0.f);
+  o[idx] = fmaxf((v - ms.x)*ms.y*g[c] + be[c], 0.f);
 }
 
 __global__ void __launch_bounds__(256) k_nbrlist(const int* __restrict__ ind,
@@ -724,7 +798,7 @@
 __global__ void __launch_bounds__(256) k_conv_gemm(
     const float* __restrict__ src, const float* __restrict__ Wc,
     const int* __restrict__ tapcnt, const int* __restrict__ ptlist,
-    const float* __restrict__ bnst, const float* __restrict__ bng,
+    const double* __restrict__ bnst, const float* __restrict__ bng,
     const float* __restrict__ bnbe, const float* __restrict__ res,
     int fmode, float* __restrict__ part){
   int tap = blockIdx.y;
@@ -733,11 +807,16 @@
   if (r0 >= n) return;
   __shared__ float Alt[96*34];
   __shared__ float Wlt[96*98];
+  __shared__ float lms[192];
   __shared__ int pqs[32];
   int tid = threadIdx.x;
   if (tid < 32){
     int r = r0 + tid;
     pqs[tid] = (r < n) ? ptlist[tap*NPTS + r] : -1;
+  }
+  if (fmode && tid < 96){
+    float2 ms = bnstat(bnst, tid);
+    lms[tid*2] = ms.x; lms[tid*2+1] = ms.y;
   }
   __syncthreads();
   for (int idx4 = tid; idx4 < 2304; idx4 += 256){
@@ -755,10 +834,10 @@
       s4 = ((const float4*)(src + (long)q*CH))[c4];
       if (fmode){
         int c0 = c4*4;
-        float vx = fmaxf((s4.x - bnst[(c0+0)*2])*bnst[(c0+0)*2+1]*bng[c0+0] + bnbe[c0+0], 0.f);
-        float vy = fmaxf((s4.y - bnst[(c0+1)*2])*bnst[(c0+1)*2+1]*bng[c0+1] + bnbe[c0+1], 0.f);
-        float vz = fmaxf((s4.z - bnst[(c0+2)*2])*bnst[(c0+2)*2+1]*bng[c0+2] + bnbe[c0+2], 0.f);
-        float vw = fmaxf((s4.w - bnst[(c0+3)*2])*bnst[(c0+3)*2+1]*bng[c0+3] + bnbe[c0+3], 0.f);
+        float vx = fmaxf((s4.x - lms[(c0+0)*2])*lms[(c0+0)*2+1]*bng[c0+0] + bnbe[c0+0], 0.f);
+        float vy = fmaxf((s4.y - lms[(c0+1)*2])*lms[(c0+1)*2+1]*bng[c0+1] + bnbe[c0+1], 0.f);
+        float vz = fmaxf((s4.z - lms[(c0+2)*2])*lms[(c0+2)*2+1]*bng[c0+2] + bnbe[c0+2], 0.f);
+        float vw = fmaxf((s4.w - lms[(c0+3)*2])*lms[(c0+3)*2+1]*bng[c0+3] + bnbe[c0+3], 0.f);
         if (fmode == 2){
           const float* rr = res + (long)q*CH + c0;
           vx += rr[0]; vy += rr[1]; vz += rr[2]; vw += rr[3];
@@ -803,8 +882,13 @@
 }
 __global__ void __launch_bounds__(256) k_conv_sum(const int* __restrict__ nbrtab,
                                                   const float* __restrict__ part,
-                                                  float* __restrict__ out){
-  int idx = blockIdx.x*256 + threadIdx.x;
+                                                  float* __restrict__ out,
+                                                  double* __restrict__ csum){
+  __shared__ float lsum[96], lsq[96];
+  int tid = threadIdx.x;
+  if (tid < 96){ lsum[tid] = 0.f; lsq[tid] = 0.f; }
+  __syncthreads();
+  int idx = blockIdx.x*256 + tid;
   int p = idx/24, c4 = idx - p*24;
   const int* nt = nbrtab + p*27;
   float4 acc = make_float4(0.f,0.f,0.f,0.f);
@@ -815,6 +899,16 @@
     }
   }
   ((float4*)out)[idx] = acc;
+  int c0 = c4*4;
+  atomicAdd(&lsum[c0+0], acc.x); atomicAdd(&lsq[c0+0], acc.x*acc.x);
+  atomicAdd(&lsum[c0+1], acc.y); atomicAdd(&lsq[c0+1], acc.y*acc.y);
+  atomicAdd(&lsum[c0+2], acc.z); atomicAdd(&lsq[c0+2], acc.z*acc.z);
+  atomicAdd(&lsum[c0+3], acc.w); atomicAdd(&lsq[c0+3], acc.w*acc.w);
+  __syncthreads();
+  if (tid < 96){
+    atomicAdd(&csum[tid*2],   (double)lsum[tid]);
+    atomicAdd(&csum[tid*2+1], (double)lsq[tid]);
+  }
 }
 __global__ void __launch_bounds__(256) k_conv_gemm_atomic(
     const float* __restrict__ src, const float* __restrict__ Wc,
@@ -876,15 +970,21 @@
     for (int j=0;j<6;++j) atomicAdd(&o[j], acc1[j]);
   }
 }
-__global__ void k_final(const float* __restrict__ c2, const float* __restrict__ st12,
+__global__ void k_final(const float* __restrict__ c2, const double* __restrict__ st12,
                         const float* __restrict__ g2, const float* __restrict__ be2,
-                        const float* __restrict__ tf, const float* __restrict__ st10,
+                        const float* __restrict__ tf, const double* __restrict__ st10,
                         const float* __restrict__ fg, const float* __restrict__ fbe,
                         const float* __restrict__ feat, float* __restrict__ out){
+  __shared__ float l10[192], l12[192];
+  if (threadIdx.x < 96){
+    float2 a = bnstat(st10, threadIdx.x); l10[threadIdx.x*2]=a.x; l10[threadIdx.x*2+1]=a.y;
+    float2 b = bnstat(st12, threadIdx.x); l12[threadIdx.x*2]=b.x; l12[threadIdx.x*2+1]=b.y;
+  }
+  __syncthreads();
   int idx = blockIdx.x*blockDim.x + threadIdx.x;
   int c = idx % CH;
-  float fsd = fmaxf((tf[idx] - st10[c*2])*st10[c*2+1]*fg[c] + fbe[c], 0.f) + feat[idx];
-  float v = (c2[idx] - st12[c*2])*st12[c*2+1]*g2[c] + be2[c];
+  float fsd = fmaxf((tf[idx] - l10[c*2])*l10[c*2+1]*fg[c] + fbe[c], 0.f) + feat[idx];
+  float v = (c2[idx] - l12[c*2])*l12[c*2+1]*g2[c] + be2[c];
   out[idx] = fmaxf(v + fsd, 0.f);
 }
 
@@ -956,18 +1056,17 @@
   size_t o_gsz    = alloc((size_t)NPTS*3*4);
   size_t o_reps   = alloc(16*4);
   size_t o_bkt    = alloc((size_t)3*100*3*4);
-  size_t o_ids    = alloc((size_t)3*NPTS*8);
   size_t o_seg    = alloc((size_t)3*NPTS*4);
   size_t o_table  = alloc((size_t)65536*4);
   size_t o_nbr    = alloc((size_t)NPTS*27*4);
   size_t o_ptlist = alloc((size_t)27*NPTS*4);
   size_t o_t64    = alloc((size_t)NPTS*64*4);
-  size_t o_stats  = alloc((size_t)13*192*4);
   size_t o_htk    = alloc((size_t)3*HTSZ*8);
   size_t o_htv    = alloc((size_t)3*HTSZ*4);
   size_t o_S      = alloc(3*FNC);
   size_t o_E      = alloc(3*FNC);
   size_t o_F      = alloc(3*FNC);
+  size_t o_stats  = alloc((size_t)13*192*8);
   size_t o_cnt    = alloc((size_t)3*NPTS*4);
   size_t o_rank   = alloc((size_t)NPTS*4);
   size_t o_tapcnt = alloc(32*4);
@@ -989,7 +1088,7 @@
   size_t o_part = alloc((size_t)NPTS*27*CH*4);
   bool use_part = (off <= ws_size);
 
-  float* stats = (float*)(ws + o_stats);
+  double* stats = (double*)(ws + o_stats);
   long zcount = (long)((zend - o_S)/4);
 
   k_setup0<<<dim3(2048), dim3(256), 0, stream>>>((int*)(ws+o_S), zcount,
@@ -998,16 +1097,14 @@
       (int*)(ws+o_start), (int*)(ws+o_table), (unsigned*)(ws+o_ball));
 
   k_mm<<<dim3(192,1), 256, 0, stream>>>(x, fp_w, fp_b, (float*)(ws+o_t9), 96, 9,
-      0,0,0,0, nullptr,0, nullptr,nullptr,0, nullptr,nullptr,nullptr, nullptr, 0);
-  k_stats<<<dim3(9,1), 256, 0, stream>>>((float*)(ws+o_t9), 0, 9, stats+0*192, 0);
-  k_p_att_enh<<<dim3(24), 256, 0, stream>>>((float*)(ws+o_t9), stats+0*192, fp_g, fp_be,
+      0,0,0,0, nullptr,0, nullptr,nullptr,0, nullptr,nullptr,nullptr, nullptr, 0, stats+0);
+  k_p_att_enh<<<dim3(24), 256, 0, stream>>>((float*)(ws+o_t9), stats+0, fp_g, fp_be,
       att_w1, att_b1, att_w2, att_b2, (float*)(ws+o_enh));
 
   k_mm<<<dim3(192,1), 256, 0, stream>>>((float*)(ws+o_enh), ff_w1, ff_b1, (float*)(ws+o_T96), 9, 96,
-      0,0,0,0, nullptr,0, nullptr,nullptr,0, nullptr,nullptr,nullptr, nullptr, 0);
-  k_stats<<<dim3(96,1), 256, 0, stream>>>((float*)(ws+o_T96), 0, 96, stats+1*192, 0);
+      0,0,0,0, nullptr,0, nullptr,nullptr,0, nullptr,nullptr,nullptr, nullptr, 0, stats+1*192);
   k_mm<<<dim3(192,1), 256, 0, stream>>>((float*)(ws+o_T96), ff_w2, ff_b2, (float*)(ws+o_fu), 96, 96,
-      0,0,0,0, stats+1*192,0, ff_g, ff_be,0, nullptr,nullptr,nullptr, nullptr, 1);
+      0,0,0,0, stats+1*192,0, ff_g, ff_be,0, nullptr,nullptr,nullptr, nullptr, 1, nullptr);
 
   k_sem_feat<<<dim3(1536), 256, 0, stream>>>((float*)(ws+o_fu), x, sa_w1, sa_b1, sa_w2, sa_b2,
       (float*)(ws+o_feat));
@@ -1016,8 +1113,7 @@
       (unsigned*)(ws+o_ball), (float*)(ws+o_dens), (float*)(ws+o_lin));
 
   k_mm<<<dim3(192,1), 256, 0, stream>>>((float*)(ws+o_feat), fj_w1, fj_b1, (float*)(ws+o_t64), 96, 64,
-      0,0,0,0, nullptr,0, nullptr,nullptr,0, nullptr,nullptr,nullptr, nullptr, 0);
-  k_stats<<<dim3(64,1), 256, 0, stream>>>((float*)(ws+o_t64), 0, 64, stats+2*192, 0);
+      0,0,0,0, nullptr,0, nullptr,nullptr,0, nullptr,nullptr,nullptr, nullptr, 0, stats+2*192);
   k_geo<<<dim3(24), 256, 0, stream>>>((float*)(ws+o_t64), stats+2*192, fj_g, fj_be, fj_w2, fj_b2,
       (float*)(ws+o_dens), (float*)(ws+o_lin), (float*)(ws+o_gsz), (float*)(ws+o_gm));
 
@@ -1025,34 +1121,29 @@
   k_scatter_reps<<<dim3(24), 256, 0, stream>>>((int*)(ws+o_rank), (float*)(ws+o_gsz),
       (float*)(ws+o_bkt), (int*)(ws+o_done), (float*)(ws+o_reps));
 
-  k_cluster<<<dim3(24,3), 256, 0, stream>>>(ind, (float*)(ws+o_reps), (int*)(ws+o_start),
-      (long long*)(ws+o_ids));
-  k_seg_build<<<dim3(24,3), 256, 0, stream>>>((long long*)(ws+o_ids),
+  k_seg_build<<<dim3(24,3), 256, 0, stream>>>(ind, (float*)(ws+o_reps), (int*)(ws+o_start),
       (unsigned long long*)(ws+o_htk), (int*)(ws+o_htv));
-  k_seg_lookup<<<dim3(24,3), 256, 0, stream>>>((long long*)(ws+o_ids),
+  k_seg_lookup<<<dim3(24,3), 256, 0, stream>>>(ind, (float*)(ws+o_reps), (int*)(ws+o_start),
       (unsigned long long*)(ws+o_htk), (int*)(ws+o_htv), (int*)(ws+o_seg), (int*)(ws+o_cnt));
 
   k_mm<<<dim3(192,3), 256, 0, stream>>>((float*)(ws+o_feat), lw_w, nullptr, (float*)(ws+o_tlw), 96, 96,
-      0, 96*96, NCELEM, 0, nullptr,0, nullptr,nullptr,0, nullptr,nullptr,nullptr, nullptr, 0);
-  k_stats<<<dim3(96,3), 256, 0, stream>>>((float*)(ws+o_tlw), NCELEM, 96, stats+3*192, 192);
+      0, 96*96, NCELEM, 0, nullptr,0, nullptr,nullptr,0, nullptr,nullptr,nullptr, nullptr, 0, stats+3*192);
   k_pw_accum<<<dim3(2304,3), 256, 0, stream>>>((float*)(ws+o_tlw), stats+3*192, lw_g, lw_be,
       (int*)(ws+o_seg), (float*)(ws+o_S));
   k_mm<<<dim3(192,3), 256, 0, stream>>>((float*)(ws+o_tlw), w_w, nullptr, (float*)(ws+o_pw2), 96, 96,
       NCELEM, 96*96, NCELEM, 0, stats+3*192,192, lw_g, lw_be,96,
-      (float*)(ws+o_S), (int*)(ws+o_seg), (int*)(ws+o_cnt), (unsigned*)(ws+o_maxenc), 2);
+      (float*)(ws+o_S), (int*)(ws+o_seg), (int*)(ws+o_cnt), (unsigned*)(ws+o_maxenc), 2, nullptr);
   k_exp_accum<<<dim3(2304,3), 256, 0, stream>>>((float*)(ws+o_pw2), (unsigned*)(ws+o_maxenc),
       (int*)(ws+o_seg), (float*)(ws+o_E));
   k_mm<<<dim3(192,4), 256, 0, stream>>>((float*)(ws+o_feat), proj_w, nullptr, (float*)(ws+o_tp), 96, 96,
-      0, 96*96, NCELEM, 0, nullptr,0, nullptr,nullptr,0, nullptr,nullptr,nullptr, nullptr, 0);
-  k_stats<<<dim3(96,4), 256, 0, stream>>>((float*)(ws+o_tp), NCELEM, 96, stats+6*192, 192);
+      0, 96*96, NCELEM, 0, nullptr,0, nullptr,nullptr,0, nullptr,nullptr,nullptr, nullptr, 0, stats+6*192);
   k_pf_accum<<<dim3(2304,3), 256, 0, stream>>>((float*)(ws+o_tp), stats+6*192, proj_g, proj_be,
       (float*)(ws+o_pw2), (unsigned*)(ws+o_maxenc), (int*)(ws+o_seg), (float*)(ws+o_E), (float*)(ws+o_F));
   k_adp_agg<<<dim3(192), 256, 0, stream>>>((float*)(ws+o_feat), adp_w, (float*)(ws+o_F),
       (int*)(ws+o_seg), (float*)(ws+o_agg));
 
   k_mm_fuse<<<dim3(192), 256, 0, stream>>>((float*)(ws+o_tp) + (size_t)3*NCELEM, stats+9*192,
-      proj_g + 3*96, proj_be + 3*96, (float*)(ws+o_agg), fuse_w, (float*)(ws+o_tf));
-  k_stats<<<dim3(96,1), 256, 0, stream>>>((float*)(ws+o_tf), 0, 96, stats+10*192, 0);
+      proj_g + 3*96, proj_be + 3*96, (float*)(ws+o_agg), fuse_w, (float*)(ws+o_tf), stats+10*192);
 
   k_nbrlist<<<dim3(24), 256, 0, stream>>>(ind, (int*)(ws+o_table), (int*)(ws+o_nbr),
       (int*)(ws+o_tapcnt), (int*)(ws+o_ptlist));
@@ -1061,13 +1152,12 @@
         (int*)(ws+o_tapcnt), (int*)(ws+o_ptlist),
         stats+10*192, fuse_g, fuse_be, (float*)(ws+o_feat), 2, (float*)(ws+o_part));
     k_conv_sum<<<dim3(NPTS*24/256), 256, 0, stream>>>((int*)(ws+o_nbr), (float*)(ws+o_part),
-        (float*)(ws+o_c1));
-    k_stats<<<dim3(96,1), 256, 0, stream>>>((float*)(ws+o_c1), 0, 96, stats+11*192, 0);
+        (float*)(ws+o_c1), stats+11*192);
     k_conv_gemm<<<dim3(192,27), 256, 0, stream>>>((float*)(ws+o_c1), conv2_w,
         (int*)(ws+o_tapcnt), (int*)(ws+o_ptlist),
         stats+11*192, bn1_g, bn1_be, nullptr, 1, (float*)(ws+o_part));
     k_conv_sum<<<dim3(NPTS*24/256), 256, 0, stream>>>((int*)(ws+o_nbr), (float*)(ws+o_part),
-        (float*)(ws+o_c2));
+        (float*)(ws+o_c2), stats+12*192);
   } else {
     k_fused<<<dim3(2304), 256, 0, stream>>>((float*)(ws+o_tf), stats+10*192, fuse_g, fuse_be,
         (float*)(ws+o_feat), (float*)(ws+o_fsd));
@@ -1080,8 +1170,8 @@
     k_zero<<<dim3(2304), dim3(256), 0, stream>>>((int*)(ws+o_c2), NCELEM);
     k_conv_gemm_atomic<<<dim3(192,27), 256, 0, stream>>>((float*)(ws+o_f1), conv2_w,
         (int*)(ws+o_tapcnt), (int*)(ws+o_ptlist), (float*)(ws+o_c2));
-  }
-  k_stats<<<dim3(96,1), 256, 0, stream>>>((float*)(ws+o_c2), 0, 96, stats+12*192, 0);
+    k_stats<<<dim3(96,1), 256, 0, stream>>>((float*)(ws+o_c2), 0, 96, stats+12*192, 0);
+  }
   k_final<<<dim3(2304), 256, 0, stream>>>((float*)(ws+o_c2), stats+12*192, bn2_g, bn2_be,
       (float*)(ws+o_tf), stats+10*192, fuse_g, fuse_be, (float*)(ws+o_feat), outp);
 }
```
